# Optimization experiments

Measured on AMD Instinct MI355X. Metric: run time of the kernel, lower is better.

The kernel has to match this reference:

```python
import jax, jax.numpy as jnp
import numpy as np

T, B, X, F, Z, H = 64, 512, 784, 64, 64, 512


def _lin(v, W, b):
    return v @ W.T + b


def _gru(xt, h, Wih, Whh, bih, bhh):
    # PyTorch GRUCell gate math
    gi = xt @ Wih.T + bih
    gh = h @ Whh.T + bhh
    ir, iz, in_ = jnp.split(gi, 3, axis=-1)
    hr, hz, hn = jnp.split(gh, 3, axis=-1)
    r = jax.nn.sigmoid(ir + hr)
    z = jax.nn.sigmoid(iz + hz)
    n = jnp.tanh(in_ + r * hn)
    return (1.0 - z) * n + z * h


def _kld(mu1, sd1, mu2, sd2):
    r = sd1 / sd2
    return 0.5 * jnp.sum(((mu1 - mu2) / sd2) ** 2 + r ** 2 - 2.0 * jnp.log(r) - 1.0)


def setup_inputs() -> dict:
    key = jax.random.key(0)
    ks = iter(jax.random.split(key, 64))

    def Wn(*shape):
        return 0.02 * jax.random.normal(next(ks), shape, jnp.float32)

    d = {}
    d["x"] = jax.random.uniform(next(ks), (T, B, X), jnp.float32)
    d["eps_f"] = jax.random.normal(next(ks), (B, F), jnp.float32)
    d["eps_z"] = jax.random.normal(next(ks), (T, B, Z), jnp.float32)
    d.update(
        pxW1=Wn(H, X), pxb1=Wn(H), pxW2=Wn(H, H), pxb2=Wn(H),
        pzW=Wn(H, Z), pzb=Wn(H),
        pfW=Wn(H, F), pfb=Wn(H),
        rWih=Wn(3 * H, 3 * H), rWhh=Wn(3 * H, H), rbih=Wn(3 * H), rbhh=Wn(3 * H),
        zpW=Wn(H, H), zpb=Wn(H), zpmW=Wn(Z, H), zpmb=Wn(Z), zpsW=Wn(Z, H), zpsb=Wn(Z),
        feWih=Wn(3 * H, H), feWhh=Wn(3 * H, H), febih=Wn(3 * H), febhh=Wn(3 * H),
        femW=Wn(F, H), femb=Wn(F), fesW=Wn(F, H), fesb=Wn(F),
        zeW1=Wn(H, 2 * H), zeb1=Wn(H), zeW2=Wn(H, H), zeb2=Wn(H),
        zemW=Wn(Z, H), zemb=Wn(Z), zesW=Wn(Z, H), zesb=Wn(Z),
        dW1=Wn(H, 3 * H), db1=Wn(H), dW2=Wn(H, H), db2=Wn(H),
        dmW=Wn(X, H), dmb=Wn(X),
    )
    return d


def reference(x, eps_f, eps_z, pxW1, pxb1, pxW2, pxb2, pzW, pzb, pfW, pfb,
              rWih, rWhh, rbih, rbhh, zpW, zpb, zpmW, zpmb, zpsW, zpsb,
              feWih, feWhh, febih, febhh, femW, femb, fesW, fesb,
              zeW1, zeb1, zeW2, zeb2, zemW, zemb, zesW, zesb,
              dW1, db1, dW2, db2, dmW, dmb):
    relu = jax.nn.relu
    # phi_x over all timesteps at once: [T, B, H]
    phi_x = relu(_lin(relu(_lin(x, pxW1, pxb1)), pxW2, pxb2))
    h0 = jnp.zeros((x.shape[1], H), x.dtype)

    # f encoder GRU over the sequence; only the final hidden is used
    f_h, _ = jax.lax.scan(
        lambda h, xt: (_gru(xt, h, feWih, feWhh, febih, febhh), None), h0, phi_x)
    f_mean = _lin(f_h, femW, femb)
    f_std = jax.nn.softplus(_lin(f_h, fesW, fesb))
    f = eps_f * f_std + f_mean
    phi_f = relu(_lin(f, pfW, pfb))
    f_kld = _kld(f_mean, f_std, jnp.zeros_like(f_mean), jnp.ones_like(f_std))

    def step(carry, inp):
        h, zk, nll = carry
        px_t, e_t, x_t = inp
        zp = relu(_lin(h, zpW, zpb))
        zpm = _lin(zp, zpmW, zpmb)
        zps = jax.nn.softplus(_lin(zp, zpsW, zpsb))
        ze = relu(_lin(relu(_lin(jnp.concatenate([px_t, h], 1), zeW1, zeb1)), zeW2, zeb2))
        zem = _lin(ze, zemW, zemb)
        zes = jax.nn.softplus(_lin(ze, zesW, zesb))
        z_t = e_t * zes + zem
        phi_z = relu(_lin(z_t, pzW, pzb))
        dec = relu(_lin(relu(_lin(jnp.concatenate([phi_z, phi_f, h], 1), dW1, db1)), dW2, db2))
        dec_mean = jax.nn.sigmoid(_lin(dec, dmW, dmb))
        h_new = _gru(jnp.concatenate([px_t, phi_z, phi_f], 1), h, rWih, rWhh, rbih, rbhh)
        zk = zk + _kld(zem, zes, zpm, zps)
        nll = nll - jnp.sum(x_t * jnp.log(dec_mean) + (1.0 - x_t) * jnp.log(1.0 - dec_mean))
        return (h_new, zk, nll), None

    zero = jnp.zeros((), x.dtype)
    (_, z_kld, nll), _ = jax.lax.scan(step, (h0, zero, zero), (phi_x, eps_z, x))
    return (f_kld, z_kld, nll)
```

## Files before the change

### kernel.cpp

```cpp
#include <hip/hip_runtime.h>
#include <cmath>

namespace {

constexpr int Tn = 64;
constexpr int Bn = 512;
constexpr int Xn = 784;
constexpr int XnP = 800;
constexpr int Fn = 64;
constexpr int Zn = 64;
constexpr int Hn = 512;

typedef unsigned short us;
typedef __attribute__((ext_vector_type(8))) short bf16x8;
typedef __attribute__((ext_vector_type(4))) float f32x4;

__device__ __forceinline__ us f2b(float v) {
  unsigned int u = __float_as_uint(v);
  return (us)((u + 0x7FFFu + ((u >> 16) & 1u)) >> 16);
}
__device__ __forceinline__ float b2f(us u) { return __uint_as_float(((unsigned int)u) << 16); }
__device__ __forceinline__ float sigmf(float v) { return 1.0f / (1.0f + __expf(-v)); }
__device__ __forceinline__ float splusf(float v) {
  return v > 0.0f ? (v + log1pf(__expf(-v))) : log1pf(__expf(v));
}
__device__ __forceinline__ float block_sum(float v, float* red) {
  #pragma unroll
  for (int off = 32; off > 0; off >>= 1) v += __shfl_down(v, off, 64);
  if ((threadIdx.x & 63) == 0) red[threadIdx.x >> 6] = v;
  __syncthreads();
  float s = 0.0f;
  if (threadIdx.x == 0) s = red[0] + red[1] + red[2] + red[3];
  return s;
}

__global__ void cvt(const float* __restrict__ s, us* __restrict__ d, int n) {
  int i = blockIdx.x * 256 + threadIdx.x;
  if (i < n) d[i] = f2b(s[i]);
}
__global__ void cvt_pad(const float* __restrict__ s, us* __restrict__ d, int C, int Cp, int n) {
  int i = blockIdx.x * 256 + threadIdx.x;
  if (i < n) {
    int r = i / Cp, c = i - r * Cp;
    d[i] = (c < C) ? f2b(s[(size_t)r * C + c]) : (us)0;
  }
}

template <int NSEG, bool RELU, bool F32OUT, bool HASINIT, bool HASBIAS>
__device__ void tile_gemmx(
    int bx, int by,
    const us* A0, const us* W0, int ldw0, int K0,
    const us* A1, const us* W1, int ldw1, int K1,
    const float* initC, int ldi, const float* bias,
    void* Cout, int ldc, char* smemc)
{
  us* As = (us*)smemc; us* Bs = (us*)(smemc + 5120);
  const int tid = threadIdx.x, srow = tid >> 2, scb = (tid & 3) * 8;
  const int lane = tid & 63, w = tid >> 6, l15 = lane & 15, q = lane >> 4;
  const int m0 = by * 64, n0 = bx * 64;
  f32x4 acc[4];
  if (HASINIT) {
    #pragma unroll
    for (int j = 0; j < 4; ++j)
      #pragma unroll
      for (int r = 0; r < 4; ++r)
        acc[j][r] = initC[(size_t)(m0 + w * 16 + q * 4 + r) * ldi + n0 + j * 16 + l15];
  } else {
    #pragma unroll
    for (int j = 0; j < 4; ++j) acc[j] = (f32x4){0.f, 0.f, 0.f, 0.f};
  }
  #pragma unroll
  for (int seg = 0; seg < NSEG; ++seg) {
    const us* A = (seg == 0) ? A0 : A1;
    const us* W = (seg == 0) ? W0 : W1;
    const int ldw = (seg == 0) ? ldw0 : ldw1;
    const int K   = (seg == 0) ? K0 : K1;
    const us* ap = A + (size_t)(m0 + srow) * K + scb;
    const us* wp = W + (size_t)(n0 + srow) * ldw + scb;
    uint4 av = *(const uint4*)ap;
    uint4 wv = *(const uint4*)wp;
    for (int k0 = 0; k0 < K; k0 += 32) {
      __syncthreads();
      *(uint4*)&As[srow * 40 + scb] = av;
      *(uint4*)&Bs[srow * 40 + scb] = wv;
      __syncthreads();
      if (k0 + 32 < K) {
        av = *(const uint4*)(ap + k0 + 32);
        wv = *(const uint4*)(wp + k0 + 32);
      }
      bf16x8 a = *(const bf16x8*)&As[(w * 16 + l15) * 40 + q * 8];
      #pragma unroll
      for (int j = 0; j < 4; ++j) {
        bf16x8 b = *(const bf16x8*)&Bs[(j * 16 + l15) * 40 + q * 8];
        acc[j] = __builtin_amdgcn_mfma_f32_16x16x32_bf16(a, b, acc[j], 0, 0, 0);
      }
    }
  }
  #pragma unroll
  for (int j = 0; j < 4; ++j) {
    const int col = n0 + j * 16 + l15;
    const float bv = HASBIAS ? bias[col] : 0.f;
    #pragma unroll
    for (int r = 0; r < 4; ++r) {
      const int row = m0 + w * 16 + q * 4 + r;
      float v = acc[j][r] + bv;
      if (RELU) v = fmaxf(v, 0.f);
      if (F32OUT) ((float*)Cout)[(size_t)row * ldc + col] = v;
      else        ((us*)Cout)[(size_t)row * ldc + col] = f2b(v);
    }
  }
}

__device__ void tile_gru_fe(
    int bx, int by,
    const us* A0, const us* Wih,
    const us* hprev, const us* Whh,
    const float* bih, const float* bhh,
    us* hnew, char* smemc)
{
  us* Asm = (us*)smemc; us* Rs = (us*)(smemc + 5120);
  us* Zs = (us*)(smemc + 10240); us* Ns = (us*)(smemc + 15360);
  const int tid = threadIdx.x, srow = tid >> 2, scb = (tid & 3) * 8;
  const int lane = tid & 63, w = tid >> 6, l15 = lane & 15, q = lane >> 4;
  const int m0 = by * 64, c0 = bx * 64;
  f32x4 aR[4], aZ[4], aI[4], aH[4];
  #pragma unroll
  for (int j = 0; j < 4; ++j) {
    aR[j] = (f32x4){0.f, 0.f, 0.f, 0.f}; aZ[j] = aR[j]; aI[j] = aR[j]; aH[j] = aR[j];
  }
  #pragma unroll
  for (int seg = 0; seg < 2; ++seg) {
    const bool hseg = (seg == 1);
    const us* A  = hseg ? hprev : A0;
    const us* Wb = hseg ? Whh : Wih;
    const us* ap = A + (size_t)(m0 + srow) * Hn + scb;
    const us* wr = Wb + (size_t)(c0 + srow) * Hn + scb;
    const us* wz = wr + (size_t)Hn * Hn;
    const us* wn = wz + (size_t)Hn * Hn;
    uint4 av = *(const uint4*)ap;
    uint4 rv = *(const uint4*)wr;
    uint4 zv = *(const uint4*)wz;
    uint4 nv = *(const uint4*)wn;
    for (int k0 = 0; k0 < Hn; k0 += 32) {
      __syncthreads();
      *(uint4*)&Asm[srow * 40 + scb] = av;
      *(uint4*)&Rs[srow * 40 + scb] = rv;
      *(uint4*)&Zs[srow * 40 + scb] = zv;
      *(uint4*)&Ns[srow * 40 + scb] = nv;
      __syncthreads();
      if (k0 + 32 < Hn) {
        av = *(const uint4*)(ap + k0 + 32);
        rv = *(const uint4*)(wr + k0 + 32);
        zv = *(const uint4*)(wz + k0 + 32);
        nv = *(const uint4*)(wn + k0 + 32);
      }
      bf16x8 a = *(const bf16x8*)&Asm[(w * 16 + l15) * 40 + q * 8];
      #pragma unroll
      for (int j = 0; j < 4; ++j) {
        bf16x8 br = *(const bf16x8*)&Rs[(j * 16 + l15) * 40 + q * 8];
        bf16x8 bz = *(const bf16x8*)&Zs[(j * 16 + l15) * 40 + q * 8];
        bf16x8 bn = *(const bf16x8*)&Ns[(j * 16 + l15) * 40 + q * 8];
        aR[j] = __builtin_amdgcn_mfma_f32_16x16x32_bf16(a, br, aR[j], 0, 0, 0);
        aZ[j] = __builtin_amdgcn_mfma_f32_16x16x32_bf16(a, bz, aZ[j], 0, 0, 0);
        if (hseg) aH[j] = __builtin_amdgcn_mfma_f32_16x16x32_bf16(a, bn, aH[j], 0, 0, 0);
        else      aI[j] = __builtin_amdgcn_mfma_f32_16x16x32_bf16(a, bn, aI[j], 0, 0, 0);
      }
    }
  }
  #pragma unroll
  for (int j = 0; j < 4; ++j) {
    const int c = c0 + j * 16 + l15;
    const float bR = bih[c] + bhh[c];
    const float bZ = bih[Hn + c] + bhh[Hn + c];
    const float bI = bih[2 * Hn + c];
    const float bH = bhh[2 * Hn + c];
    #pragma unroll
    for (int r = 0; r < 4; ++r) {
      const int m = m0 + w * 16 + q * 4 + r;
      const float h = b2f(hprev[(size_t)m * Hn + c]);
      const float rg = sigmf(aR[j][r] + bR);
      const float zg = sigmf(aZ[j][r] + bZ);
      const float ng = tanhf(aI[j][r] + bI + rg * (aH[j][r] + bH));
      hnew[(size_t)m * Hn + c] = f2b((1.0f - zg) * ng + zg * h);
    }
  }
}

__device__ void tile_gru_fin(
    int bx, int by,
    const us* phiz, const us* rWih,
    const float* gipre, const float* ghpre,
    const us* hprev,
    const float* bih, const float* bhh,
    us* hnew, char* smemc)
{
  us* Asm = (us*)smemc; us* Rs = (us*)(smemc + 5120);
  us* Zs = (us*)(smemc + 10240); us* Ns = (us*)(smemc + 15360);
  const int tid = threadIdx.x, srow = tid >> 2, scb = (tid & 3) * 8;
  const int lane = tid & 63, w = tid >> 6, l15 = lane & 15, q = lane >> 4;
  const int m0 = by * 64, c0 = bx * 64;
  f32x4 aR[4], aZ[4], aI[4];
  float aH[4][4];
  #pragma unroll
  for (int j = 0; j < 4; ++j) {
    const int c = c0 + j * 16 + l15;
    #pragma unroll
    for (int r = 0; r < 4; ++r) {
      const size_t row = (size_t)(m0 + w * 16 + q * 4 + r) * 1536;
      aR[j][r] = gipre[row + c] + ghpre[row + c];
      aZ[j][r] = gipre[row + 512 + c] + ghpre[row + 512 + c];
      aI[j][r] = gipre[row + 1024 + c];
      aH[j][r] = ghpre[row + 1024 + c];
    }
  }
  const us* ap = phiz + (size_t)(m0 + srow) * Hn + scb;
  const us* wr = rWih + (size_t)(c0 + srow) * 1536 + 512 + scb;
  const us* wz = wr + (size_t)512 * 1536;
  const us* wn = wz + (size_t)512 * 1536;
  uint4 av = *(const uint4*)ap;
  uint4 rv = *(const uint4*)wr;
  uint4 zv = *(const uint4*)wz;
  uint4 nv = *(const uint4*)wn;
  for (int k0 = 0; k0 < Hn; k0 += 32) {
    __syncthreads();
    *(uint4*)&Asm[srow * 40 + scb] = av;
    *(uint4*)&Rs[srow * 40 + scb] = rv;
    *(uint4*)&Zs[srow * 40 + scb] = zv;
    *(uint4*)&Ns[srow * 40 + scb] = nv;
    __syncthreads();
    if (k0 + 32 < Hn) {
      av = *(const uint4*)(ap + k0 + 32);
      rv = *(const uint4*)(wr + k0 + 32);
      zv = *(const uint4*)(wz + k0 + 32);
      nv = *(const uint4*)(wn + k0 + 32);
    }
    bf16x8 a = *(const bf16x8*)&Asm[(w * 16 + l15) * 40 + q * 8];
    #pragma unroll
    for (int j = 0; j < 4; ++j) {
      bf16x8 br = *(const bf16x8*)&Rs[(j * 16 + l15) * 40 + q * 8];
      bf16x8 bz = *(const bf16x8*)&Zs[(j * 16 + l15) * 40 + q * 8];
      bf16x8 bn = *(const bf16x8*)&Ns[(j * 16 + l15) * 40 + q * 8];
      aR[j] = __builtin_amdgcn_mfma_f32_16x16x32_bf16(a, br, aR[j], 0, 0, 0);
      aZ[j] = __builtin_amdgcn_mfma_f32_16x16x32_bf16(a, bz, aZ[j], 0, 0, 0);
      aI[j] = __builtin_amdgcn_mfma_f32_16x16x32_bf16(a, bn, aI[j], 0, 0, 0);
    }
  }
  #pragma unroll
  for (int j = 0; j < 4; ++j) {
    const int c = c0 + j * 16 + l15;
    const float bR = bih[c] + bhh[c];
    const float bZ = bih[Hn + c] + bhh[Hn + c];
    const float bI = bih[2 * Hn + c];
    const float bH = bhh[2 * Hn + c];
    #pragma unroll
    for (int r = 0; r < 4; ++r) {
      const int m = m0 + w * 16 + q * 4 + r;
      const float h = b2f(hprev[(size_t)m * Hn + c]);
      const float rg = sigmf(aR[j][r] + bR);
      const float zg = sigmf(aZ[j][r] + bZ);
      const float ng = tanhf(aI[j][r] + bI + rg * (aH[j][r] + bH));
      hnew[(size_t)m * Hn + c] = f2b((1.0f - zg) * ng + zg * h);
    }
  }
}

__device__ void tile_nll(
    int bx, int by,
    const us* dec, const us* dmW, const float* dmb, const float* xt,
    float* nll, char* smemc)
{
  us* As = (us*)smemc; us* Bs = (us*)(smemc + 5120);
  float* red = (float*)(smemc + 10240);
  const int tid = threadIdx.x, srow = tid >> 2, scb = (tid & 3) * 8;
  const int lane = tid & 63, w = tid >> 6, l15 = lane & 15, q = lane >> 4;
  const int m0 = by * 64, n0 = bx * 64;
  f32x4 acc[4];
  #pragma unroll
  for (int j = 0; j < 4; ++j) acc[j] = (f32x4){0.f, 0.f, 0.f, 0.f};
  const int wrow = (n0 + srow < Xn) ? (n0 + srow) : (Xn - 1);
  const us* ap = dec + (size_t)(m0 + srow) * Hn + scb;
  const us* wp = dmW + (size_t)wrow * Hn + scb;
  uint4 av = *(const uint4*)ap;
  uint4 wv = *(const uint4*)wp;
  for (int k0 = 0; k0 < Hn; k0 += 32) {
    __syncthreads();
    *(uint4*)&As[srow * 40 + scb] = av;
    *(uint4*)&Bs[srow * 40 + scb] = wv;
    __syncthreads();
    if (k0 + 32 < Hn) {
      av = *(const uint4*)(ap + k0 + 32);
      wv = *(const uint4*)(wp + k0 + 32);
    }
    bf16x8 a = *(const bf16x8*)&As[(w * 16 + l15) * 40 + q * 8];
    #pragma unroll
    for (int j = 0; j < 4; ++j) {
      bf16x8 b = *(const bf16x8*)&Bs[(j * 16 + l15) * 40 + q * 8];
      acc[j] = __builtin_amdgcn_mfma_f32_16x16x32_bf16(a, b, acc[j], 0, 0, 0);
    }
  }
  float sum = 0.0f;
  #pragma unroll
  for (int j = 0; j < 4; ++j) {
    const int n = n0 + j * 16 + l15;
    if (n < Xn) {
      const float bv = dmb[n];
      #pragma unroll
      for (int r = 0; r < 4; ++r) {
        const int m = m0 + w * 16 + q * 4 + r;
        const float a = acc[j][r] + bv;
        const float xv = xt[(size_t)m * Xn + n];
        sum += splusf(-a) + (1.0f - xv) * a;
      }
    }
  }
  const float s = block_sum(sum, red);
  if (tid == 0) atomicAdd(nll, s);
}

template <int MODE>
__device__ void stat_dual(int vb,
    const us* Ain, const us* Wm, const float* bm, const us* Ws, const float* bs,
    const float* eps, const float* pm_in, const float* ps_in,
    us* o0b, float* o_pm, float* o_ps, float* kacc, char* smemc)
{
  us* As = (us*)smemc; us* Ms = (us*)(smemc + 5120); us* Ss = (us*)(smemc + 10240);
  float* red = (float*)(smemc + 15360);
  const int tid = threadIdx.x, srow = tid >> 2, scb = (tid & 3) * 8;
  const int lane = tid & 63, w = tid >> 6, l15 = lane & 15, q = lane >> 4;
  const int m0 = vb * 64;
  f32x4 am[4], as_[4];
  #pragma unroll
  for (int j = 0; j < 4; ++j) { am[j] = (f32x4){0.f, 0.f, 0.f, 0.f}; as_[j] = am[j]; }
  const us* ap = Ain + (size_t)(m0 + srow) * Hn + scb;
  const us* mp = Wm + (size_t)srow * Hn + scb;
  const us* sp = Ws + (size_t)srow * Hn + scb;
  uint4 av = *(const uint4*)ap;
  uint4 mv = *(const uint4*)mp;
  uint4 sv = *(const uint4*)sp;
  for (int k0 = 0; k0 < Hn; k0 += 32) {
    __syncthreads();
    *(uint4*)&As[srow * 40 + scb] = av;
    *(uint4*)&Ms[srow * 40 + scb] = mv;
    *(uint4*)&Ss[srow * 40 + scb] = sv;
    __syncthreads();
    if (k0 + 32 < Hn) {
      av = *(const uint4*)(ap + k0 + 32);
      mv = *(const uint4*)(mp + k0 + 32);
      sv = *(const uint4*)(sp + k0 + 32);
    }
    bf16x8 a = *(const bf16x8*)&As[(w * 16 + l15) * 40 + q * 8];
    #pragma unroll
    for (int j = 0; j < 4; ++j) {
      bf16x8 b0 = *(const bf16x8*)&Ms[(j * 16 + l15) * 40 + q * 8];
      bf16x8 b1 = *(const bf16x8*)&Ss[(j * 16 + l15) * 40 + q * 8];
      am[j]  = __builtin_amdgcn_mfma_f32_16x16x32_bf16(a, b0, am[j], 0, 0, 0);
      as_[j] = __builtin_amdgcn_mfma_f32_16x16x32_bf16(a, b1, as_[j], 0, 0, 0);
    }
  }
  float kld = 0.0f;
  #pragma unroll
  for (int j = 0; j < 4; ++j) {
    const int c = j * 16 + l15;
    const float bmv = bm[c], bsv = bs[c];
    #pragma unroll
    for (int r = 0; r < 4; ++r) {
      const int m = m0 + w * 16 + q * 4 + r;
      const float mu = am[j][r] + bmv;
      const float sd = splusf(as_[j][r] + bsv);
      if (MODE == 0) {
        o_pm[(size_t)m * Zn + c] = mu;
        o_ps[(size_t)m * Zn + c] = sd;
      } else {
        o0b[(size_t)m * Zn + c] = f2b(eps[(size_t)m * Zn + c] * sd + mu);
        if (MODE == 1) {
          kld += mu * mu + sd * sd - 2.0f * __logf(sd) - 1.0f;
        } else {
          const float pm = pm_in[(size_t)m * Zn + c];
          const float ps = ps_in[(size_t)m * Zn + c];
          const float dd = (mu - pm) / ps;
          const float rr = sd / ps;
          kld += dd * dd + rr * rr - 2.0f * __logf(rr) - 1.0f;
        }
      }
    }
  }
  if (MODE != 0) {
    const float s = block_sum(kld, red);
    if (tid == 0) atomicAdd(kacc, 0.5f * s);
  }
}

__global__ __launch_bounds__(256) void k_gemmA(
    const us* A, const us* W, int ldw, int K, const float* bias, us* C, int ldc)
{
  __shared__ alignas(16) char sm[10240];
  tile_gemmx<1, true, false, false, true>(blockIdx.x, blockIdx.y, A, W, ldw, K,
      nullptr, nullptr, 0, 0, nullptr, 0, bias, C, ldc, sm);
}

__global__ __launch_bounds__(256) void k_gruB(
    const us* A0, const us* Wih, const us* hprev, const us* Whh,
    const float* bih, const float* bhh, us* hnew)
{
  __shared__ alignas(16) char sm[20480];
  tile_gru_fe(blockIdx.x, blockIdx.y, A0, Wih, hprev, Whh, bih, bhh, hnew, sm);
}

__global__ __launch_bounds__(256) void k_statf(
    const us* fh, const us* femW, const float* femb, const us* fesW, const float* fesb,
    const float* eps_f, us* fbuf, float* kacc)
{
  __shared__ alignas(16) char sm[15376];
  stat_dual<1>(blockIdx.x, fh, femW, femb, fesW, fesb, eps_f,
               nullptr, nullptr, fbuf, nullptr, nullptr, kacc, sm);
}

__global__ __launch_bounds__(256) void kP2(
    const us* phi_f, const us* rWih, const us* dW1, const float* db1,
    float* Cpre_gru, float* Cpre_dec)
{
  __shared__ alignas(16) char sm[10240];
  const int b = blockIdx.x;
  if (b < 192)
    tile_gemmx<1, false, true, false, false>(b % 24, b / 24, phi_f, rWih + 1024, 1536, Hn,
        nullptr, nullptr, 0, 0, nullptr, 0, nullptr, Cpre_gru, 1536, sm);
  else
    tile_gemmx<1, false, true, false, true>((b - 192) & 7, (b - 192) >> 3,
        phi_f, dW1 + 512, 1536, Hn,
        nullptr, nullptr, 0, 0, nullptr, 0, db1, Cpre_dec, 512, sm);
}

__global__ __launch_bounds__(256) void kP3(
    const us* h0, const us* zpW, const float* zpb, us* zp,
    const us* px0, const us* zeW1, const float* zeb1, us* zepre)
{
  __shared__ alignas(16) char sm[10240];
  const int b = blockIdx.x;
  if (b < 64)
    tile_gemmx<1, true, false, false, true>(b & 7, b >> 3, h0, zpW, Hn, Hn,
        nullptr, nullptr, 0, 0, nullptr, 0, zpb, zp, Hn, sm);
  else
    tile_gemmx<2, true, false, false, true>((b - 64) & 7, (b - 64) >> 3,
        px0, zeW1, 1024, Hn, h0, zeW1 + 512, 1024, Hn,
        nullptr, 0, zeb1, zepre, Hn, sm);
}

__global__ __launch_bounds__(256) void kP4(
    const us* zepre, const us* zeW2, const float* zeb2, us* ze,
    const us* zp, const us* zpmW, const float* zpmb, const us* zpsW, const float* zpsb,
    float* zpm, float* zps)
{
  __shared__ alignas(16) char sm[15376];
  const int b = blockIdx.x;
  if (b < 64)
    tile_gemmx<1, true, false, false, true>(b & 7, b >> 3, zepre, zeW2, Hn, Hn,
        nullptr, nullptr, 0, 0, nullptr, 0, zeb2, ze, Hn, sm);
  else
    stat_dual<0>(b - 64, zp, zpmW, zpmb, zpsW, zpsb,
                 nullptr, nullptr, nullptr, nullptr, zpm, zps, nullptr, sm);
}

__global__ __launch_bounds__(256) void kS1(
    const us* ze, const us* zemW, const float* zemb, const us* zesW, const float* zesb,
    const float* eps_zt, const float* zpm, const float* zps, us* zt, float* kacc,
    const us* px_t, const us* rWih, const float* Cpre_gru, float* gipre)
{
  __shared__ alignas(16) char sm[15376];
  const int b = blockIdx.x;
  if (b < 8)
    stat_dual<2>(b, ze, zemW, zemb, zesW, zesb, eps_zt, zpm, zps,
                 zt, nullptr, nullptr, kacc, sm);
  else {
    const int tb = b - 8;
    tile_gemmx<1, false, true, true, false>(tb % 24, tb / 24, px_t, rWih, 1536, Hn,
        nullptr, nullptr, 0, 0, Cpre_gru, 1536, nullptr, gipre, 1536, sm);
  }
}

__global__ __launch_bounds__(256) void kS2(
    const us* zt, const us* pzW, const float* pzb, us* phiz)
{
  __shared__ alignas(16) char sm[10240];
  tile_gemmx<1, true, false, false, true>(blockIdx.x & 7, blockIdx.x >> 3, zt, pzW, Zn, Zn,
      nullptr, nullptr, 0, 0, nullptr, 0, pzb, phiz, Hn, sm);
}

__global__ __launch_bounds__(256) void kS3(
    const us* phiz, const us* rWih, const float* gipre, const float* ghpre,
    const us* hprev, const float* rbih, const float* rbhh, us* hnew,
    const us* dW1, const float* dtmph, us* dtmp)
{
  __shared__ alignas(16) char sm[20480];
  const int b = blockIdx.x;
  if (b < 64)
    tile_gru_fin(b & 7, b >> 3, phiz, rWih, gipre, ghpre, hprev, rbih, rbhh, hnew, sm);
  else
    tile_gemmx<1, true, false, true, false>((b - 64) & 7, (b - 64) >> 3, phiz, dW1, 1536, Hn,
        nullptr, nullptr, 0, 0, dtmph, 512, nullptr, dtmp, Hn, sm);
}

__global__ __launch_bounds__(256) void kS4(
    const us* dtmp, const us* dW2, const float* db2, us* dec,
    const us* hnext, const us* zpW, const float* zpb, us* zp,
    const us* px1, const us* zeW1, const float* zeb1, us* zepre,
    const us* dW1, const float* Cpre_dec, float* dtmph)
{
  __shared__ alignas(16) char sm[10240];
  const int b = blockIdx.x;
  if (b < 64)
    tile_gemmx<1, true, false, false, true>(b & 7, b >> 3, dtmp, dW2, Hn, Hn,
        nullptr, nullptr, 0, 0, nullptr, 0, db2, dec, Hn, sm);
  else if (b < 128)
    tile_gemmx<1, true, false, false, true>((b - 64) & 7, (b - 64) >> 3, hnext, zpW, Hn, Hn,
        nullptr, nullptr, 0, 0, nullptr, 0, zpb, zp, Hn, sm);
  else if (b < 192)
    tile_gemmx<2, true, false, false, true>((b - 128) & 7, (b - 128) >> 3,
        px1, zeW1, 1024, Hn, hnext, zeW1 + 512, 1024, Hn,
        nullptr, 0, zeb1, zepre, Hn, sm);
  else
    tile_gemmx<1, false, true, true, false>((b - 192) & 7, (b - 192) >> 3,
        hnext, dW1 + 1024, 1536, Hn,
        nullptr, nullptr, 0, 0, Cpre_dec, 512, nullptr, dtmph, 512, sm);
}

__global__ __launch_bounds__(256) void kS5(
    const us* dec, const us* dmW, const float* dmb, const float* xt, float* nll,
    const us* zepre, const us* zeW2, const float* zeb2, us* ze,
    const us* zp, const us* zpmW, const float* zpmb, const us* zpsW, const float* zpsb,
    float* zpm, float* zps,
    const us* hnext, const us* rWhh, float* ghpre)
{
  __shared__ alignas(16) char sm[15376];
  const int b = blockIdx.x;
  if (b < 104)
    tile_nll(b % 13, b / 13, dec, dmW, dmb, xt, nll, sm);
  else if (b < 168)
    tile_gemmx<1, true, false, false, true>((b - 104) & 7, (b - 104) >> 3, zepre, zeW2, Hn, Hn,
        nullptr, nullptr, 0, 0, nullptr, 0, zeb2, ze, Hn, sm);
  else if (b < 176)
    stat_dual<0>(b - 168, zp, zpmW, zpmb, zpsW, zpsb,
                 nullptr, nullptr, nullptr, nullptr, zpm, zps, nullptr, sm);
  else {
    const int tb = b - 176;
    tile_gemmx<1, false, true, false, false>(tb % 24, tb / 24, hnext, rWhh, Hn, Hn,
        nullptr, nullptr, 0, 0, nullptr, 0, nullptr, ghpre, 1536, sm);
  }
}

}

extern "C" void kernel_launch(void* const* d_in, const int* in_sizes, int n_in,
                              void* d_out, int out_size, void* d_ws, size_t ws_size,
                              hipStream_t stream)
{
  (void)in_sizes; (void)n_in; (void)out_size;
  const float* x     = (const float*)d_in[0];
  const float* eps_f = (const float*)d_in[1];
  const float* eps_z = (const float*)d_in[2];
  const float* pxW1  = (const float*)d_in[3];
  const float* pxb1  = (const float*)d_in[4];
  const float* pxW2  = (const float*)d_in[5];
  const float* pxb2  = (const float*)d_in[6];
  const float* pzW   = (const float*)d_in[7];
  const float* pzb   = (const float*)d_in[8];
  const float* pfW   = (const float*)d_in[9];
  const float* pfb   = (const float*)d_in[10];
  const float* rWih  = (const float*)d_in[11];
  const float* rWhh  = (const float*)d_in[12];
  const float* rbih  = (const float*)d_in[13];
  const float* rbhh  = (const float*)d_in[14];
  const float* zpW   = (const float*)d_in[15];
  const float* zpb   = (const float*)d_in[16];
  const float* zpmW  = (const float*)d_in[17];
  const float* zpmb  = (const float*)d_in[18];
  const float* zpsW  = (const float*)d_in[19];
  const float* zpsb  = (const float*)d_in[20];
  const float* feWih = (const float*)d_in[21];
  const float* feWhh = (const float*)d_in[22];
  const float* febih = (const float*)d_in[23];
  const float* febhh = (const float*)d_in[24];
  const float* femW  = (const float*)d_in[25];
  const float* femb  = (const float*)d_in[26];
  const float* fesW  = (const float*)d_in[27];
  const float* fesb  = (const float*)d_in[28];
  const float* zeW1  = (const float*)d_in[29];
  const float* zeb1  = (const float*)d_in[30];
  const float* zeW2  = (const float*)d_in[31];
  const float* zeb2  = (const float*)d_in[32];
  const float* zemW  = (const float*)d_in[33];
  const float* zemb  = (const float*)d_in[34];
  const float* zesW  = (const float*)d_in[35];
  const float* zesb  = (const float*)d_in[36];
  const float* dW1   = (const float*)d_in[37];
  const float* db1   = (const float*)d_in[38];
  const float* dW2   = (const float*)d_in[39];
  const float* db2   = (const float*)d_in[40];
  const float* dmW   = (const float*)d_in[41];
  const float* dmb   = (const float*)d_in[42];
  float* out = (float*)d_out;

  char* base = (char*)d_ws;
  size_t off = 0;
  auto ab = [&](size_t bytes) -> void* {
    void* p = base + off;
    off += (bytes + 255) & ~(size_t)255;
    return p;
  };

  us* b_pxW1  = (us*)ab((size_t)512 * XnP * 2);
  us* b_pxW2  = (us*)ab((size_t)512 * 512 * 2);
  us* b_pzW   = (us*)ab((size_t)512 * 64 * 2);
  us* b_pfW   = (us*)ab((size_t)512 * 64 * 2);
  us* b_rWih  = (us*)ab((size_t)1536 * 1536 * 2);
  us* b_rWhh  = (us*)ab((size_t)1536 * 512 * 2);
  us* b_zpW   = (us*)ab((size_t)512 * 512 * 2);
  us* b_zpmW  = (us*)ab((size_t)64 * 512 * 2);
  us* b_zpsW  = (us*)ab((size_t)64 * 512 * 2);
  us* b_feWih = (us*)ab((size_t)1536 * 512 * 2);
  us* b_feWhh = (us*)ab((size_t)1536 * 512 * 2);
  us* b_femW  = (us*)ab((size_t)64 * 512 * 2);
  us* b_fesW  = (us*)ab((size_t)64 * 512 * 2);
  us* b_zeW1  = (us*)ab((size_t)512 * 1024 * 2);
  us* b_zeW2  = (us*)ab((size_t)512 * 512 * 2);
  us* b_zemW  = (us*)ab((size_t)64 * 512 * 2);
  us* b_zesW  = (us*)ab((size_t)64 * 512 * 2);
  us* b_dW1   = (us*)ab((size_t)512 * 1536 * 2);
  us* b_dW2   = (us*)ab((size_t)512 * 512 * 2);
  us* b_dmW   = (us*)ab((size_t)Xn * 512 * 2);

  us* phi_x = (us*)ab((size_t)Tn * Bn * Hn * 2);
  us* fh_a  = (us*)ab((size_t)Bn * Hn * 2);
  us* h_a   = (us*)ab((size_t)Bn * Hn * 2);
  us* fh_b  = (us*)ab((size_t)Bn * Hn * 2);
  us* h_b   = (us*)ab((size_t)Bn * Hn * 2);
  us* fbuf  = (us*)ab((size_t)Bn * Fn * 2);
  us* phi_f = (us*)ab((size_t)Bn * Hn * 2);
  us* zp    = (us*)ab((size_t)Bn * Hn * 2);
  us* zepre = (us*)ab((size_t)Bn * Hn * 2);
  us* ze    = (us*)ab((size_t)Bn * Hn * 2);
  us* zt    = (us*)ab((size_t)Bn * Zn * 2);
  us* phiz  = (us*)ab((size_t)Bn * Hn * 2);
  us* dtmp  = (us*)ab((size_t)Bn * Hn * 2);
  us* dec   = (us*)ab((size_t)Bn * Hn * 2);
  float* zpm = (float*)ab((size_t)Bn * Zn * 4);
  float* zps = (float*)ab((size_t)Bn * Zn * 4);
  float* Cpre_gru = (float*)ab((size_t)Bn * 1536 * 4);
  float* Cpre_dec = (float*)ab((size_t)Bn * 512 * 4);
  float* gipre    = (float*)ab((size_t)Bn * 1536 * 4);
  float* ghpre    = (float*)ab((size_t)Bn * 1536 * 4);
  float* dtmph    = (float*)ab((size_t)Bn * 512 * 4);

  int CH = 16;
  while (CH > 1 && off + (size_t)CH * (Bn * XnP + Bn * Hn) * 2 + 4096 > ws_size) CH >>= 1;
  us* xch  = (us*)ab((size_t)CH * Bn * XnP * 2);
  us* tmpb = (us*)ab((size_t)CH * Bn * Hn * 2);

  hipMemsetAsync(d_out, 0, 3 * sizeof(float), stream);
  hipMemsetAsync(fh_a, 0, 2 * (size_t)Bn * Hn * 2, stream);
  hipMemsetAsync(ghpre, 0, (size_t)Bn * 1536 * 4, stream);

  const dim3 blk(256);
  auto CVT = [&](const float* s, us* d, size_t n) {
    cvt<<<dim3((unsigned)((n + 255) / 256)), blk, 0, stream>>>(s, d, (int)n);
  };

  {
    const size_t n = (size_t)512 * XnP;
    cvt_pad<<<dim3((unsigned)((n + 255) / 256)), blk, 0, stream>>>(pxW1, b_pxW1, Xn, XnP, (int)n);
  }
  CVT(pxW2, b_pxW2, (size_t)512 * 512);
  CVT(pzW, b_pzW, (size_t)512 * 64);
  CVT(pfW, b_pfW, (size_t)512 * 64);
  CVT(rWih, b_rWih, (size_t)1536 * 1536);
  CVT(rWhh, b_rWhh, (size_t)1536 * 512);
  CVT(zpW, b_zpW, (size_t)512 * 512);
  CVT(zpmW, b_zpmW, (size_t)64 * 512);
  CVT(zpsW, b_zpsW, (size_t)64 * 512);
  CVT(feWih, b_feWih, (size_t)1536 * 512);
  CVT(feWhh, b_feWhh, (size_t)1536 * 512);
  CVT(femW, b_femW, (size_t)64 * 512);
  CVT(fesW, b_fesW, (size_t)64 * 512);
  CVT(zeW1, b_zeW1, (size_t)512 * 1024);
  CVT(zeW2, b_zeW2, (size_t)512 * 512);
  CVT(zemW, b_zemW, (size_t)64 * 512);
  CVT(zesW, b_zesW, (size_t)64 * 512);
  CVT(dW1, b_dW1, (size_t)512 * 1536);
  CVT(dW2, b_dW2, (size_t)512 * 512);
  CVT(dmW, b_dmW, (size_t)Xn * 512);

  for (int c = 0; c < Tn / CH; ++c) {
    const size_t nx = (size_t)CH * Bn * XnP;
    cvt_pad<<<dim3((unsigned)((nx + 255) / 256)), blk, 0, stream>>>(
        x + (size_t)c * CH * Bn * Xn, xch, Xn, XnP, (int)nx);
    const dim3 gA(8, CH * Bn / 64);
    k_gemmA<<<gA, blk, 0, stream>>>(xch, b_pxW1, XnP, XnP, pxb1, tmpb, Hn);
    k_gemmA<<<gA, blk, 0, stream>>>(tmpb, b_pxW2, Hn, Hn, pxb2,
                                    phi_x + (size_t)c * CH * Bn * Hn, Hn);
  }

  us* fc = fh_a; us* fn2 = fh_b;
  for (int t = 0; t < Tn; ++t) {
    k_gruB<<<dim3(8, 8), blk, 0, stream>>>(
        phi_x + (size_t)t * Bn * Hn, b_feWih, fc, b_feWhh, febih, febhh, fn2);
    us* sw = fc; fc = fn2; fn2 = sw;
  }

  k_statf<<<dim3(8), blk, 0, stream>>>(fh_a, b_femW, femb, b_fesW, fesb, eps_f, fbuf, out + 0);

  k_gemmA<<<dim3(8, 8), blk, 0, stream>>>(fbuf, b_pfW, Fn, Fn, pfb, phi_f, Hn);
  kP2<<<dim3(256), blk, 0, stream>>>(phi_f, b_rWih, b_dW1, db1, Cpre_gru, Cpre_dec);
  hipMemcpyAsync(dtmph, Cpre_dec, (size_t)Bn * 512 * 4, hipMemcpyDeviceToDevice, stream);
  kP3<<<dim3(128), blk, 0, stream>>>(h_a, b_zpW, zpb, zp, phi_x, b_zeW1, zeb1, zepre);
  kP4<<<dim3(72), blk, 0, stream>>>(zepre, b_zeW2, zeb2, ze,
                                    zp, b_zpmW, zpmb, b_zpsW, zpsb, zpm, zps);

  for (int t = 0; t < Tn; ++t) {
    const us* hcur = (t & 1) ? h_b : h_a;
    us* hnext      = (t & 1) ? h_a : h_b;
    const bool last = (t == Tn - 1);
    const us* px_t = phi_x + (size_t)t * Bn * Hn;

    kS1<<<dim3(200), blk, 0, stream>>>(
        ze, b_zemW, zemb, b_zesW, zesb, eps_z + (size_t)t * Bn * Zn, zpm, zps,
        zt, out + 1, px_t, b_rWih, Cpre_gru, gipre);

    kS2<<<dim3(64), blk, 0, stream>>>(zt, b_pzW, pzb, phiz);

    kS3<<<dim3(128), blk, 0, stream>>>(
        phiz, b_rWih, gipre, ghpre, hcur, rbih, rbhh, hnext,
        b_dW1, dtmph, dtmp);

    kS4<<<dim3(last ? 64 : 256), blk, 0, stream>>>(
        dtmp, b_dW2, db2, dec,
        hnext, b_zpW, zpb, zp,
        phi_x + (size_t)(t + 1) * Bn * Hn, b_zeW1, zeb1, zepre,
        b_dW1, Cpre_dec, dtmph);

    kS5<<<dim3(last ? 104 : 368), blk, 0, stream>>>(
        dec, b_dmW, dmb, x + (size_t)t * Bn * Xn, out + 2,
        zepre, b_zeW2, zeb2, ze,
        zp, b_zpmW, zpmb, b_zpsW, zpsb, zpm, zps,
        hnext, b_rWhh, ghpre);
  }
}
```

Before: 6.594 ms.

## Replace per-step kernel launches with a single cooperative persistent megakernel

Folds the weight conversion, phi_x GEMMs, f-encoder GRU and the whole 64-step recurrence into one cooperative kernel of 256 blocks. Grid-wide syncs replace the hundreds of separate kernel launches. The GRU is split so the input-side gate GEMM is precomputed separately from the hidden-side GEMM. The NLL reconstruction term is moved out of the recurrence into one batched kernel over all timesteps, which appears to reuse the phi_x buffer to hold the decoder outputs. Grid.sync cost and the fixed one-block-per-CU occupancy could offset the removed launch overhead.

After: 16.11 ms. 2.44x slower.

```diff
diff --git a/kernel.cpp b/kernel.cpp
--- a/kernel.cpp
+++ b/kernel.cpp
@@ -1,5 +1,8 @@
 #include <hip/hip_runtime.h>
+#include <hip/hip_cooperative_groups.h>
 #include <cmath>
+
+namespace cg = cooperative_groups;
 
 namespace {
 
@@ -10,6 +13,8 @@
 constexpr int Fn = 64;
 constexpr int Zn = 64;
 constexpr int Hn = 512;
+constexpr int NB = 256;
+constexpr int NTH = 256;
 
 typedef unsigned short us;
 typedef __attribute__((ext_vector_type(8))) short bf16x8;
@@ -34,17 +39,27 @@
   return s;
 }
 
-__global__ void cvt(const float* __restrict__ s, us* __restrict__ d, int n) {
-  int i = blockIdx.x * 256 + threadIdx.x;
-  if (i < n) d[i] = f2b(s[i]);
-}
-__global__ void cvt_pad(const float* __restrict__ s, us* __restrict__ d, int C, int Cp, int n) {
-  int i = blockIdx.x * 256 + threadIdx.x;
-  if (i < n) {
-    int r = i / Cp, c = i - r * Cp;
-    d[i] = (c < C) ? f2b(s[(size_t)r * C + c]) : (us)0;
-  }
-}
+struct KParams {
+  const float *x, *eps_f, *eps_z;
+  const float *f_pxW1, *pxb1, *f_pxW2, *pxb2;
+  const float *f_pzW, *pzb, *f_pfW, *pfb;
+  const float *f_rWih, *f_rWhh, *rbih, *rbhh;
+  const float *f_zpW, *zpb, *f_zpmW, *zpmb, *f_zpsW, *zpsb;
+  const float *f_feWih, *f_feWhh, *febih, *febhh;
+  const float *f_femW, *femb, *f_fesW, *fesb;
+  const float *f_zeW1, *zeb1, *f_zeW2, *zeb2, *f_zemW, *zemb, *f_zesW, *zesb;
+  const float *f_dW1, *db1, *f_dW2, *db2, *f_dmW, *dmb;
+  float* out;
+  us *b_pxW1, *b_pxW2, *b_pzW, *b_pfW, *b_rWih, *b_rWhh, *b_zpW, *b_zpmW, *b_zpsW;
+  us *b_feWih, *b_feWhh, *b_femW, *b_fesW, *b_zeW1, *b_zeW2, *b_zemW, *b_zesW;
+  us *b_dW1, *b_dW2, *b_dmW;
+  us *phi_x, *fh_a, *fh_b, *fbuf, *phi_f, *h_a, *h_b;
+  us *zp, *zepre, *ze, *phiz, *dtmp, *dec;
+  float *zpm, *zps, *Cpre_gru, *Cpre_dec, *gipre, *ghpre, *dtmph;
+  float *parts;
+  us *xch, *tmpb;
+  int CH;
+};
 
 template <int NSEG, bool RELU, bool F32OUT, bool HASINIT, bool HASBIAS>
 __device__ void tile_gemmx(
@@ -111,60 +126,122 @@
   }
 }
 
-__device__ void tile_gru_fe(
-    int bx, int by,
-    const us* A0, const us* Wih,
-    const us* hprev, const us* Whh,
-    const float* bih, const float* bhh,
-    us* hnew, char* smemc)
+template <bool HASINIT>
+__device__ void tile_g3(int bx, int by, const us* A, const us* W, int ldw,
+                        const float* initC, float* outC, char* smemc)
 {
   us* Asm = (us*)smemc; us* Rs = (us*)(smemc + 5120);
   us* Zs = (us*)(smemc + 10240); us* Ns = (us*)(smemc + 15360);
   const int tid = threadIdx.x, srow = tid >> 2, scb = (tid & 3) * 8;
   const int lane = tid & 63, w = tid >> 6, l15 = lane & 15, q = lane >> 4;
   const int m0 = by * 64, c0 = bx * 64;
-  f32x4 aR[4], aZ[4], aI[4], aH[4];
+  f32x4 aR[4], aZ[4], aN[4];
+  if (HASINIT) {
+    #pragma unroll
+    for (int j = 0; j < 4; ++j) {
+      const int c = c0 + j * 16 + l15;
+      #pragma unroll
+      for (int r = 0; r < 4; ++r) {
+        const size_t row = (size_t)(m0 + w * 16 + q * 4 + r) * 1536;
+        aR[j][r] = initC[row + c];
+        aZ[j][r] = initC[row + 512 + c];
+        aN[j][r] = initC[row + 1024 + c];
+      }
+    }
+  } else {
+    #pragma unroll
+    for (int j = 0; j < 4; ++j) {
+      aR[j] = (f32x4){0.f, 0.f, 0.f, 0.f}; aZ[j] = aR[j]; aN[j] = aR[j];
+    }
+  }
+  const us* ap = A + (size_t)(m0 + srow) * Hn + scb;
+  const us* wr = W + (size_t)(c0 + srow) * ldw + scb;
+  const us* wz = wr + (size_t)512 * ldw;
+  const us* wn = wz + (size_t)512 * ldw;
+  uint4 av = *(const uint4*)ap;
+  uint4 rv = *(const uint4*)wr;
+  uint4 zv = *(const uint4*)wz;
+  uint4 nv = *(const uint4*)wn;
+  for (int k0 = 0; k0 < Hn; k0 += 32) {
+    __syncthreads();
+    *(uint4*)&Asm[srow * 40 + scb] = av;
+    *(uint4*)&Rs[srow * 40 + scb] = rv;
+    *(uint4*)&Zs[srow * 40 + scb] = zv;
+    *(uint4*)&Ns[srow * 40 + scb] = nv;
+    __syncthreads();
+    if (k0 + 32 < Hn) {
+      av = *(const uint4*)(ap + k0 + 32);
+      rv = *(const uint4*)(wr + k0 + 32);
+      zv = *(const uint4*)(wz + k0 + 32);
+      nv = *(const uint4*)(wn + k0 + 32);
+    }
+    bf16x8 a = *(const bf16x8*)&Asm[(w * 16 + l15) * 40 + q * 8];
+    #pragma unroll
+    for (int j = 0; j < 4; ++j) {
+      bf16x8 br = *(const bf16x8*)&Rs[(j * 16 + l15) * 40 + q * 8];
+      bf16x8 bz = *(const bf16x8*)&Zs[(j * 16 + l15) * 40 + q * 8];
+      bf16x8 bn = *(const bf16x8*)&Ns[(j * 16 + l15) * 40 + q * 8];
+      aR[j] = __builtin_amdgcn_mfma_f32_16x16x32_bf16(a, br, aR[j], 0, 0, 0);
+      aZ[j] = __builtin_amdgcn_mfma_f32_16x16x32_bf16(a, bz, aZ[j], 0, 0, 0);
+      aN[j] = __builtin_amdgcn_mfma_f32_16x16x32_bf16(a, bn, aN[j], 0, 0, 0);
+    }
+  }
   #pragma unroll
   for (int j = 0; j < 4; ++j) {
-    aR[j] = (f32x4){0.f, 0.f, 0.f, 0.f}; aZ[j] = aR[j]; aI[j] = aR[j]; aH[j] = aR[j];
-  }
-  #pragma unroll
-  for (int seg = 0; seg < 2; ++seg) {
-    const bool hseg = (seg == 1);
-    const us* A  = hseg ? hprev : A0;
-    const us* Wb = hseg ? Whh : Wih;
-    const us* ap = A + (size_t)(m0 + srow) * Hn + scb;
-    const us* wr = Wb + (size_t)(c0 + srow) * Hn + scb;
-    const us* wz = wr + (size_t)Hn * Hn;
-    const us* wn = wz + (size_t)Hn * Hn;
-    uint4 av = *(const uint4*)ap;
-    uint4 rv = *(const uint4*)wr;
-    uint4 zv = *(const uint4*)wz;
-    uint4 nv = *(const uint4*)wn;
-    for (int k0 = 0; k0 < Hn; k0 += 32) {
-      __syncthreads();
-      *(uint4*)&Asm[srow * 40 + scb] = av;
-      *(uint4*)&Rs[srow * 40 + scb] = rv;
-      *(uint4*)&Zs[srow * 40 + scb] = zv;
-      *(uint4*)&Ns[srow * 40 + scb] = nv;
-      __syncthreads();
-      if (k0 + 32 < Hn) {
-        av = *(const uint4*)(ap + k0 + 32);
-        rv = *(const uint4*)(wr + k0 + 32);
-        zv = *(const uint4*)(wz + k0 + 32);
-        nv = *(const uint4*)(wn + k0 + 32);
-      }
-      bf16x8 a = *(const bf16x8*)&Asm[(w * 16 + l15) * 40 + q * 8];
-      #pragma unroll
-      for (int j = 0; j < 4; ++j) {
-        bf16x8 br = *(const bf16x8*)&Rs[(j * 16 + l15) * 40 + q * 8];
-        bf16x8 bz = *(const bf16x8*)&Zs[(j * 16 + l15) * 40 + q * 8];
-        bf16x8 bn = *(const bf16x8*)&Ns[(j * 16 + l15) * 40 + q * 8];
-        aR[j] = __builtin_amdgcn_mfma_f32_16x16x32_bf16(a, br, aR[j], 0, 0, 0);
-        aZ[j] = __builtin_amdgcn_mfma_f32_16x16x32_bf16(a, bz, aZ[j], 0, 0, 0);
-        if (hseg) aH[j] = __builtin_amdgcn_mfma_f32_16x16x32_bf16(a, bn, aH[j], 0, 0, 0);
-        else      aI[j] = __builtin_amdgcn_mfma_f32_16x16x32_bf16(a, bn, aI[j], 0, 0, 0);
-      }
+    const int c = c0 + j * 16 + l15;
+    #pragma unroll
+    for (int r = 0; r < 4; ++r) {
+      const size_t row = (size_t)(m0 + w * 16 + q * 4 + r) * 1536;
+      outC[row + c] = aR[j][r];
+      outC[row + 512 + c] = aZ[j][r];
+      outC[row + 1024 + c] = aN[j][r];
+    }
+  }
+}
+
+__device__ void tile_ghgates(int bx, int by, const us* hprev, const us* Whh,
+    const float* gi, const float* bih, const float* bhh, us* hnew, char* smemc)
+{
+  us* Asm = (us*)smemc; us* Rs = (us*)(smemc + 5120);
+  us* Zs = (us*)(smemc + 10240); us* Ns = (us*)(smemc + 15360);
+  const int tid = threadIdx.x, srow = tid >> 2, scb = (tid & 3) * 8;
+  const int lane = tid & 63, w = tid >> 6, l15 = lane & 15, q = lane >> 4;
+  const int m0 = by * 64, c0 = bx * 64;
+  f32x4 aR[4], aZ[4], aH[4];
+  #pragma unroll
+  for (int j = 0; j < 4; ++j) {
+    aR[j] = (f32x4){0.f, 0.f, 0.f, 0.f}; aZ[j] = aR[j]; aH[j] = aR[j];
+  }
+  const us* ap = hprev + (size_t)(m0 + srow) * Hn + scb;
+  const us* wr = Whh + (size_t)(c0 + srow) * Hn + scb;
+  const us* wz = wr + (size_t)512 * Hn;
+  const us* wn = wz + (size_t)512 * Hn;
+  uint4 av = *(const uint4*)ap;
+  uint4 rv = *(const uint4*)wr;
+  uint4 zv = *(const uint4*)wz;
+  uint4 nv = *(const uint4*)wn;
+  for (int k0 = 0; k0 < Hn; k0 += 32) {
+    __syncthreads();
+    *(uint4*)&Asm[srow * 40 + scb] = av;
+    *(uint4*)&Rs[srow * 40 + scb] = rv;
+    *(uint4*)&Zs[srow * 40 + scb] = zv;
+    *(uint4*)&Ns[srow * 40 + scb] = nv;
+    __syncthreads();
+    if (k0 + 32 < Hn) {
+      av = *(const uint4*)(ap + k0 + 32);
+      rv = *(const uint4*)(wr + k0 + 32);
+      zv = *(const uint4*)(wz + k0 + 32);
+      nv = *(const uint4*)(wn + k0 + 32);
+    }
+    bf16x8 a = *(const bf16x8*)&Asm[(w * 16 + l15) * 40 + q * 8];
+    #pragma unroll
+    for (int j = 0; j < 4; ++j) {
+      bf16x8 br = *(const bf16x8*)&Rs[(j * 16 + l15) * 40 + q * 8];
+      bf16x8 bz = *(const bf16x8*)&Zs[(j * 16 + l15) * 40 + q * 8];
+      bf16x8 bn = *(const bf16x8*)&Ns[(j * 16 + l15) * 40 + q * 8];
+      aR[j] = __builtin_amdgcn_mfma_f32_16x16x32_bf16(a, br, aR[j], 0, 0, 0);
+      aZ[j] = __builtin_amdgcn_mfma_f32_16x16x32_bf16(a, bz, aZ[j], 0, 0, 0);
+      aH[j] = __builtin_amdgcn_mfma_f32_16x16x32_bf16(a, bn, aH[j], 0, 0, 0);
     }
   }
   #pragma unroll
@@ -177,10 +254,11 @@
     #pragma unroll
     for (int r = 0; r < 4; ++r) {
       const int m = m0 + w * 16 + q * 4 + r;
+      const size_t grow = (size_t)m * 1536;
       const float h = b2f(hprev[(size_t)m * Hn + c]);
-      const float rg = sigmf(aR[j][r] + bR);
-      const float zg = sigmf(aZ[j][r] + bZ);
-      const float ng = tanhf(aI[j][r] + bI + rg * (aH[j][r] + bH));
+      const float rg = sigmf(gi[grow + c] + aR[j][r] + bR);
+      const float zg = sigmf(gi[grow + 512 + c] + aZ[j][r] + bZ);
+      const float ng = tanhf(gi[grow + 1024 + c] + bI + rg * (aH[j][r] + bH));
       hnew[(size_t)m * Hn + c] = f2b((1.0f - zg) * ng + zg * h);
     }
   }
@@ -264,11 +342,356 @@
   }
 }
 
-__device__ void tile_nll(
-    int bx, int by,
-    const us* dec, const us* dmW, const float* dmb, const float* xt,
-    float* nll, char* smemc)
+template <int MODE>
+__device__ float stat_dual(int vb,
+    const us* Ain, const us* Wm, const float* bm, const us* Ws, const float* bs,
+    const float* eps,
+    us* o0b, float* o_pm, float* o_ps, char* smemc)
 {
+  us* As = (us*)smemc; us* Ms = (us*)(smemc + 5120); us* Ss = (us*)(smemc + 10240);
+  float* red = (float*)(smemc + 15360);
+  const int tid = threadIdx.x, srow = tid >> 2, scb = (tid & 3) * 8;
+  const int lane = tid & 63, w = tid >> 6, l15 = lane & 15, q = lane >> 4;
+  const int m0 = vb * 64;
+  f32x4 am[4], as_[4];
+  #pragma unroll
+  for (int j = 0; j < 4; ++j) { am[j] = (f32x4){0.f, 0.f, 0.f, 0.f}; as_[j] = am[j]; }
+  const us* ap = Ain + (size_t)(m0 + srow) * Hn + scb;
+  const us* mp = Wm + (size_t)srow * Hn + scb;
+  const us* sp = Ws + (size_t)srow * Hn + scb;
+  uint4 av = *(const uint4*)ap;
+  uint4 mv = *(const uint4*)mp;
+  uint4 sv = *(const uint4*)sp;
+  for (int k0 = 0; k0 < Hn; k0 += 32) {
+    __syncthreads();
+    *(uint4*)&As[srow * 40 + scb] = av;
+    *(uint4*)&Ms[srow * 40 + scb] = mv;
+    *(uint4*)&Ss[srow * 40 + scb] = sv;
+    __syncthreads();
+    if (k0 + 32 < Hn) {
+      av = *(const uint4*)(ap + k0 + 32);
+      mv = *(const uint4*)(mp + k0 + 32);
+      sv = *(const uint4*)(sp + k0 + 32);
+    }
+    bf16x8 a = *(const bf16x8*)&As[(w * 16 + l15) * 40 + q * 8];
+    #pragma unroll
+    for (int j = 0; j < 4; ++j) {
+      bf16x8 b0 = *(const bf16x8*)&Ms[(j * 16 + l15) * 40 + q * 8];
+      bf16x8 b1 = *(const bf16x8*)&Ss[(j * 16 + l15) * 40 + q * 8];
+      am[j]  = __builtin_amdgcn_mfma_f32_16x16x32_bf16(a, b0, am[j], 0, 0, 0);
+      as_[j] = __builtin_amdgcn_mfma_f32_16x16x32_bf16(a, b1, as_[j], 0, 0, 0);
+    }
+  }
+  float kld = 0.0f;
+  #pragma unroll
+  for (int j = 0; j < 4; ++j) {
+    const int c = j * 16 + l15;
+    const float bmv = bm[c], bsv = bs[c];
+    #pragma unroll
+    for (int r = 0; r < 4; ++r) {
+      const int m = m0 + w * 16 + q * 4 + r;
+      const float mu = am[j][r] + bmv;
+      const float sd = splusf(as_[j][r] + bsv);
+      if (MODE == 0) {
+        o_pm[(size_t)m * Zn + c] = mu;
+        o_ps[(size_t)m * Zn + c] = sd;
+      } else {
+        o0b[(size_t)m * Zn + c] = f2b(eps[(size_t)m * Zn + c] * sd + mu);
+        kld += mu * mu + sd * sd - 2.0f * __logf(sd) - 1.0f;
+      }
+    }
+  }
+  if (MODE != 0) return 0.5f * block_sum(kld, red);
+  return 0.0f;
+}
+
+__device__ float tile_zestat_phiz(int vb,
+    const us* ze, const us* Wm, const float* bm, const us* Ws, const float* bs,
+    const float* eps, const float* pm_in, const float* ps_in,
+    const us* pzW, const float* pzb, us* phiz,
+    char* smemc)
+{
+  us* As = (us*)smemc; us* Ms = (us*)(smemc + 5120); us* Ss = (us*)(smemc + 10240);
+  float* red = (float*)(smemc + 15360);
+  const int tid = threadIdx.x, srow = tid >> 2, scb = (tid & 3) * 8;
+  const int lane = tid & 63, w = tid >> 6, l15 = lane & 15, q = lane >> 4;
+  const int m0 = vb * 64;
+  f32x4 am[4], as_[4];
+  #pragma unroll
+  for (int j = 0; j < 4; ++j) { am[j] = (f32x4){0.f, 0.f, 0.f, 0.f}; as_[j] = am[j]; }
+  const us* ap = ze + (size_t)(m0 + srow) * Hn + scb;
+  const us* mp = Wm + (size_t)srow * Hn + scb;
+  const us* sp = Ws + (size_t)srow * Hn + scb;
+  uint4 av = *(const uint4*)ap;
+  uint4 mv = *(const uint4*)mp;
+  uint4 sv = *(const uint4*)sp;
+  for (int k0 = 0; k0 < Hn; k0 += 32) {
+    __syncthreads();
+    *(uint4*)&As[srow * 40 + scb] = av;
+    *(uint4*)&Ms[srow * 40 + scb] = mv;
+    *(uint4*)&Ss[srow * 40 + scb] = sv;
+    __syncthreads();
+    if (k0 + 32 < Hn) {
+      av = *(const uint4*)(ap + k0 + 32);
+      mv = *(const uint4*)(mp + k0 + 32);
+      sv = *(const uint4*)(sp + k0 + 32);
+    }
+    bf16x8 a = *(const bf16x8*)&As[(w * 16 + l15) * 40 + q * 8];
+    #pragma unroll
+    for (int j = 0; j < 4; ++j) {
+      bf16x8 b0 = *(const bf16x8*)&Ms[(j * 16 + l15) * 40 + q * 8];
+      bf16x8 b1 = *(const bf16x8*)&Ss[(j * 16 + l15) * 40 + q * 8];
+      am[j]  = __builtin_amdgcn_mfma_f32_16x16x32_bf16(a, b0, am[j], 0, 0, 0);
+      as_[j] = __builtin_amdgcn_mfma_f32_16x16x32_bf16(a, b1, as_[j], 0, 0, 0);
+    }
+  }
+  float kld = 0.0f;
+  us ztv[4][4];
+  #pragma unroll
+  for (int j = 0; j < 4; ++j) {
+    const int c = j * 16 + l15;
+    const float bmv = bm[c], bsv = bs[c];
+    #pragma unroll
+    for (int r = 0; r < 4; ++r) {
+      const int m = m0 + w * 16 + q * 4 + r;
+      const float mu = am[j][r] + bmv;
+      const float sd = splusf(as_[j][r] + bsv);
+      ztv[j][r] = f2b(eps[(size_t)m * Zn + c] * sd + mu);
+      const float pm = pm_in[(size_t)m * Zn + c];
+      const float ps = ps_in[(size_t)m * Zn + c];
+      const float dd = (mu - pm) / ps;
+      const float rr = sd / ps;
+      kld += dd * dd + rr * rr - 2.0f * __logf(rr) - 1.0f;
+    }
+  }
+  const float kout = 0.5f * block_sum(kld, red);
+  us* zts = (us*)smemc;
+  us* Bs = (us*)(smemc + 10240);
+  #pragma unroll
+  for (int j = 0; j < 4; ++j)
+    #pragma unroll
+    for (int r = 0; r < 4; ++r)
+      zts[(w * 16 + q * 4 + r) * 72 + (j * 16 + l15)] = ztv[j][r];
+  for (int nt = 0; nt < 8; ++nt) {
+    f32x4 pa[4];
+    #pragma unroll
+    for (int j = 0; j < 4; ++j) pa[j] = (f32x4){0.f, 0.f, 0.f, 0.f};
+    const us* wp = pzW + (size_t)(nt * 64 + srow) * 64 + scb;
+    uint4 wv = *(const uint4*)wp;
+    for (int k0 = 0; k0 < 64; k0 += 32) {
+      __syncthreads();
+      *(uint4*)&Bs[srow * 40 + scb] = wv;
+      __syncthreads();
+      if (k0 == 0) wv = *(const uint4*)(wp + 32);
+      bf16x8 a = *(const bf16x8*)&zts[(w * 16 + l15) * 72 + k0 + q * 8];
+      #pragma unroll
+      for (int j = 0; j < 4; ++j) {
+        bf16x8 b = *(const bf16x8*)&Bs[(j * 16 + l15) * 40 + q * 8];
+        pa[j] = __builtin_amdgcn_mfma_f32_16x16x32_bf16(a, b, pa[j], 0, 0, 0);
+      }
+    }
+    #pragma unroll
+    for (int j = 0; j < 4; ++j) {
+      const int col = nt * 64 + j * 16 + l15;
+      const float bv = pzb[col];
+      #pragma unroll
+      for (int r = 0; r < 4; ++r) {
+        const int row = m0 + w * 16 + q * 4 + r;
+        phiz[(size_t)row * Hn + col] = f2b(fmaxf(pa[j][r] + bv, 0.f));
+      }
+    }
+  }
+  return kout;
+}
+
+__global__ __launch_bounds__(NTH, 1) void k_mega(KParams p)
+{
+  cg::grid_group grid = cg::this_grid();
+  __shared__ alignas(16) char sm[20496];
+  const int bid = blockIdx.x;
+  const int gtid = bid * NTH + threadIdx.x;
+  const int gnt = NB * NTH;
+
+  {
+    const float* srcs[19] = {p.f_pxW2, p.f_pzW, p.f_pfW, p.f_rWih, p.f_rWhh,
+        p.f_zpW, p.f_zpmW, p.f_zpsW, p.f_feWih, p.f_feWhh, p.f_femW, p.f_fesW,
+        p.f_zeW1, p.f_zeW2, p.f_zemW, p.f_zesW, p.f_dW1, p.f_dW2, p.f_dmW};
+    us* dsts[19] = {p.b_pxW2, p.b_pzW, p.b_pfW, p.b_rWih, p.b_rWhh,
+        p.b_zpW, p.b_zpmW, p.b_zpsW, p.b_feWih, p.b_feWhh, p.b_femW, p.b_fesW,
+        p.b_zeW1, p.b_zeW2, p.b_zemW, p.b_zesW, p.b_dW1, p.b_dW2, p.b_dmW};
+    const int ns[19] = {512*512, 512*64, 512*64, 1536*1536, 1536*512,
+        512*512, 64*512, 64*512, 1536*512, 1536*512, 64*512, 64*512,
+        512*1024, 512*512, 64*512, 64*512, 512*1536, 512*512, 784*512};
+    for (int k = 0; k < 19; ++k) {
+      const float* s = srcs[k]; us* d = dsts[k]; const int n = ns[k];
+      for (int i = gtid; i < n; i += gnt) d[i] = f2b(s[i]);
+    }
+  }
+  for (int i = gtid; i < 512 * XnP; i += gnt) {
+    const int r = i / XnP, c = i - r * XnP;
+    p.b_pxW1[i] = (c < Xn) ? f2b(p.f_pxW1[(size_t)r * Xn + c]) : (us)0;
+  }
+  for (int i = gtid; i < Bn * Hn; i += gnt) { p.fh_a[i] = 0; p.h_a[i] = 0; }
+  for (int i = gtid; i < Bn * 1536; i += gnt) p.ghpre[i] = 0.f;
+  grid.sync();
+
+  const int CH = p.CH;
+  const int nch = Tn / CH;
+  for (int c = 0; c < nch; ++c) {
+    const int nx = CH * Bn * XnP;
+    const float* xsrc = p.x + (size_t)c * CH * Bn * Xn;
+    for (int i = gtid; i < nx; i += gnt) {
+      const int r = i / XnP, cc = i - r * XnP;
+      p.xch[i] = (cc < Xn) ? f2b(xsrc[(size_t)r * Xn + cc]) : (us)0;
+    }
+    grid.sync();
+    const int ntile = (CH * Bn / 64) * 8;
+    for (int tl = bid; tl < ntile; tl += NB)
+      tile_gemmx<1, true, false, false, true>(tl & 7, tl >> 3, p.xch, p.b_pxW1,
+          XnP, XnP, nullptr, nullptr, 0, 0, nullptr, 0, p.pxb1, p.tmpb, Hn, sm);
+    grid.sync();
+    for (int tl = bid; tl < ntile; tl += NB)
+      tile_gemmx<1, true, false, false, true>(tl & 7, tl >> 3, p.tmpb, p.b_pxW2,
+          Hn, Hn, nullptr, nullptr, 0, 0, nullptr, 0, p.pxb2,
+          p.phi_x + (size_t)c * CH * Bn * Hn, Hn, sm);
+    grid.sync();
+  }
+
+  float* giA = p.Cpre_gru;
+  float* giB = p.gipre;
+  if (bid < 64)
+    tile_g3<false>(bid & 7, bid >> 3, p.phi_x, p.b_feWih, Hn, nullptr, giA, sm);
+  grid.sync();
+  for (int t = 0; t < Tn; ++t) {
+    const us* hc = (t & 1) ? p.fh_b : p.fh_a;
+    us* hn = (t & 1) ? p.fh_a : p.fh_b;
+    const float* gic = (t & 1) ? giB : giA;
+    float* gin = (t & 1) ? giA : giB;
+    if (bid < 64)
+      tile_ghgates(bid & 7, bid >> 3, hc, p.b_feWhh, gic, p.febih, p.febhh, hn, sm);
+    else if (bid < 128 && t + 1 < Tn)
+      tile_g3<false>((bid - 64) & 7, (bid - 64) >> 3,
+          p.phi_x + (size_t)(t + 1) * Bn * Hn, p.b_feWih, Hn, nullptr, gin, sm);
+    grid.sync();
+  }
+
+  if (bid < 8) {
+    const float fk = stat_dual<1>(bid, p.fh_a, p.b_femW, p.femb, p.b_fesW, p.fesb,
+                                  p.eps_f, p.fbuf, nullptr, nullptr, sm);
+    if (threadIdx.x == 0) p.parts[8 + bid] = fk;
+  } else if (bid < 72)
+    tile_gemmx<1, true, false, false, true>((bid - 8) & 7, (bid - 8) >> 3,
+        p.phi_x, p.b_zeW1, 1024, Hn, nullptr, nullptr, 0, 0,
+        nullptr, 0, p.zeb1, p.zepre, Hn, sm);
+  else {
+    for (int i = (bid - 72) * NTH + threadIdx.x; i < Bn * Hn; i += (NB - 72) * NTH)
+      p.zp[i] = f2b(fmaxf(p.zpb[i & (Hn - 1)], 0.f));
+  }
+  grid.sync();
+
+  if (bid < 64)
+    tile_gemmx<1, true, false, false, true>(bid & 7, bid >> 3, p.fbuf, p.b_pfW,
+        Fn, Fn, nullptr, nullptr, 0, 0, nullptr, 0, p.pfb, p.phi_f, Hn, sm);
+  else if (bid < 128)
+    tile_gemmx<1, true, false, false, true>((bid - 64) & 7, (bid - 64) >> 3,
+        p.zepre, p.b_zeW2, Hn, Hn, nullptr, nullptr, 0, 0,
+        nullptr, 0, p.zeb2, p.ze, Hn, sm);
+  else if (bid < 136)
+    stat_dual<0>(bid - 128, p.zp, p.b_zpmW, p.zpmb, p.b_zpsW, p.zpsb, nullptr,
+                 nullptr, p.zpm, p.zps, sm);
+  grid.sync();
+
+  if (bid < 64)
+    tile_g3<false>(bid & 7, bid >> 3, p.phi_f, p.b_rWih + 1024, 1536,
+                   nullptr, p.Cpre_gru, sm);
+  else if (bid < 128)
+    tile_gemmx<1, false, true, false, true>((bid - 64) & 7, (bid - 64) >> 3,
+        p.phi_f, p.b_dW1 + 512, 1536, Hn, nullptr, nullptr, 0, 0,
+        nullptr, 0, p.db1, p.Cpre_dec, 512, sm);
+  grid.sync();
+
+  float accZ = 0.f;
+  for (int t = 0; t < Tn; ++t) {
+    const us* hc = (t & 1) ? p.h_b : p.h_a;
+    us* hn = (t & 1) ? p.h_a : p.h_b;
+    const us* px_t = p.phi_x + (size_t)t * Bn * Hn;
+
+    if (bid < 8)
+      accZ += tile_zestat_phiz(bid, p.ze, p.b_zemW, p.zemb, p.b_zesW, p.zesb,
+          p.eps_z + (size_t)t * Bn * Zn, p.zpm, p.zps,
+          p.b_pzW, p.pzb, p.phiz, sm);
+    else if (bid < 72)
+      tile_g3<true>((bid - 8) & 7, (bid - 8) >> 3, px_t, p.b_rWih, 1536,
+                    p.Cpre_gru, p.gipre, sm);
+    grid.sync();
+
+    if (bid < 64)
+      tile_gru_fin(bid & 7, bid >> 3, p.phiz, p.b_rWih, p.gipre, p.ghpre, hc,
+                   p.rbih, p.rbhh, hn, sm);
+    else if (bid < 128)
+      tile_gemmx<1, true, false, true, false>((bid - 64) & 7, (bid - 64) >> 3,
+          p.phiz, p.b_dW1, 1536, Hn, nullptr, nullptr, 0, 0,
+          (t == 0 ? p.Cpre_dec : p.dtmph), 512, nullptr, p.dtmp, Hn, sm);
+    grid.sync();
+
+    if (bid < 64)
+      tile_gemmx<1, true, false, false, true>(bid & 7, bid >> 3, p.dtmp, p.b_dW2,
+          Hn, Hn, nullptr, nullptr, 0, 0, nullptr, 0, p.db2,
+          p.phi_x + (size_t)t * Bn * Hn, Hn, sm);
+    else if (bid < 128) {
+      if (t + 1 < Tn)
+        tile_gemmx<1, true, false, false, true>((bid - 64) & 7, (bid - 64) >> 3,
+            hn, p.b_zpW, Hn, Hn, nullptr, nullptr, 0, 0,
+            nullptr, 0, p.zpb, p.zp, Hn, sm);
+    } else if (bid < 192) {
+      if (t + 1 < Tn)
+        tile_gemmx<2, true, false, false, true>((bid - 128) & 7, (bid - 128) >> 3,
+            p.phi_x + (size_t)(t + 1) * Bn * Hn, p.b_zeW1, 1024, Hn,
+            hn, p.b_zeW1 + 512, 1024, Hn,
+            nullptr, 0, p.zeb1, p.zepre, Hn, sm);
+    } else {
+      if (t + 1 < Tn)
+        tile_gemmx<1, false, true, true, false>((bid - 192) & 7, (bid - 192) >> 3,
+            hn, p.b_dW1 + 1024, 1536, Hn, nullptr, nullptr, 0, 0,
+            p.Cpre_dec, 512, nullptr, p.dtmph, 512, sm);
+    }
+    grid.sync();
+
+    if (t + 1 < Tn) {
+      if (bid < 64)
+        tile_gemmx<1, true, false, false, true>(bid & 7, bid >> 3, p.zepre,
+            p.b_zeW2, Hn, Hn, nullptr, nullptr, 0, 0,
+            nullptr, 0, p.zeb2, p.ze, Hn, sm);
+      else if (bid < 72)
+        stat_dual<0>(bid - 64, p.zp, p.b_zpmW, p.zpmb, p.b_zpsW, p.zpsb, nullptr,
+                     nullptr, p.zpm, p.zps, sm);
+      else if (bid < 136)
+        tile_g3<false>((bid - 72) & 7, (bid - 72) >> 3, hn, p.b_rWhh, Hn,
+                       nullptr, p.ghpre, sm);
+    }
+    grid.sync();
+  }
+
+  if (threadIdx.x == 0 && bid < 8) p.parts[bid] = accZ;
+  grid.sync();
+  if (bid == 0 && threadIdx.x == 0) {
+    float f = 0.f, z = 0.f;
+    for (int i = 0; i < 8; ++i) { z += p.parts[i]; f += p.parts[8 + i]; }
+    p.out[0] = f; p.out[1] = z;
+  }
+}
+
+__global__ __launch_bounds__(NTH) void k_nll_all(
+    const us* dec_all, const us* dmW, const float* dmb, const float* x, float* nll)
+{
+  __shared__ alignas(16) char smemc[10256];
+  const int b = blockIdx.x;
+  const int t = b / 104;
+  const int i = b - t * 104;
+  const int bx = i % 13, by = i / 13;
+  const us* dec = dec_all + (size_t)t * Bn * Hn;
+  const float* xt = x + (size_t)t * Bn * Xn;
+
   us* As = (us*)smemc; us* Bs = (us*)(smemc + 5120);
   float* red = (float*)(smemc + 10240);
   const int tid = threadIdx.x, srow = tid >> 2, scb = (tid & 3) * 8;
@@ -294,8 +717,8 @@
     bf16x8 a = *(const bf16x8*)&As[(w * 16 + l15) * 40 + q * 8];
     #pragma unroll
     for (int j = 0; j < 4; ++j) {
-      bf16x8 b = *(const bf16x8*)&Bs[(j * 16 + l15) * 40 + q * 8];
-      acc[j] = __builtin_amdgcn_mfma_f32_16x16x32_bf16(a, b, acc[j], 0, 0, 0);
+      bf16x8 bb = *(const bf16x8*)&Bs[(j * 16 + l15) * 40 + q * 8];
+      acc[j] = __builtin_amdgcn_mfma_f32_16x16x32_bf16(a, bb, acc[j], 0, 0, 0);
     }
   }
   float sum = 0.0f;
@@ -317,236 +740,6 @@
   if (tid == 0) atomicAdd(nll, s);
 }
 
-template <int MODE>
-__device__ void stat_dual(int vb,
-    const us* Ain, const us* Wm, const float* bm, const us* Ws, const float* bs,
-    const float* eps, const float* pm_in, const float* ps_in,
-    us* o0b, float* o_pm, float* o_ps, float* kacc, char* smemc)
-{
-  us* As = (us*)smemc; us* Ms = (us*)(smemc + 5120); us* Ss = (us*)(smemc + 10240);
-  float* red = (float*)(smemc + 15360);
-  const int tid = threadIdx.x, srow = tid >> 2, scb = (tid & 3) * 8;
-  const int lane = tid & 63, w = tid >> 6, l15 = lane & 15, q = lane >> 4;
-  const int m0 = vb * 64;
-  f32x4 am[4], as_[4];
-  #pragma unroll
-  for (int j = 0; j < 4; ++j) { am[j] = (f32x4){0.f, 0.f, 0.f, 0.f}; as_[j] = am[j]; }
-  const us* ap = Ain + (size_t)(m0 + srow) * Hn + scb;
-  const us* mp = Wm + (size_t)srow * Hn + scb;
-  const us* sp = Ws + (size_t)srow * Hn + scb;
-  uint4 av = *(const uint4*)ap;
-  uint4 mv = *(const uint4*)mp;
-  uint4 sv = *(const uint4*)sp;
-  for (int k0 = 0; k0 < Hn; k0 += 32) {
-    __syncthreads();
-    *(uint4*)&As[srow * 40 + scb] = av;
-    *(uint4*)&Ms[srow * 40 + scb] = mv;
-    *(uint4*)&Ss[srow * 40 + scb] = sv;
-    __syncthreads();
-    if (k0 + 32 < Hn) {
-      av = *(const uint4*)(ap + k0 + 32);
-      mv = *(const uint4*)(mp + k0 + 32);
-      sv = *(const uint4*)(sp + k0 + 32);
-    }
-    bf16x8 a = *(const bf16x8*)&As[(w * 16 + l15) * 40 + q * 8];
-    #pragma unroll
-    for (int j = 0; j < 4; ++j) {
-      bf16x8 b0 = *(const bf16x8*)&Ms[(j * 16 + l15) * 40 + q * 8];
-      bf16x8 b1 = *(const bf16x8*)&Ss[(j * 16 + l15) * 40 + q * 8];
-      am[j]  = __builtin_amdgcn_mfma_f32_16x16x32_bf16(a, b0, am[j], 0, 0, 0);
-      as_[j] = __builtin_amdgcn_mfma_f32_16x16x32_bf16(a, b1, as_[j], 0, 0, 0);
-    }
-  }
-  float kld = 0.0f;
-  #pragma unroll
-  for (int j = 0; j < 4; ++j) {
-    const int c = j * 16 + l15;
-    const float bmv = bm[c], bsv = bs[c];
-    #pragma unroll
-    for (int r = 0; r < 4; ++r) {
-      const int m = m0 + w * 16 + q * 4 + r;
-      const float mu = am[j][r] + bmv;
-      const float sd = splusf(as_[j][r] + bsv);
-      if (MODE == 0) {
-        o_pm[(size_t)m * Zn + c] = mu;
-        o_ps[(size_t)m * Zn + c] = sd;
-      } else {
-        o0b[(size_t)m * Zn + c] = f2b(eps[(size_t)m * Zn + c] * sd + mu);
-        if (MODE == 1) {
-          kld += mu * mu + sd * sd - 2.0f * __logf(sd) - 1.0f;
-        } else {
-          const float pm = pm_in[(size_t)m * Zn + c];
-          const float ps = ps_in[(size_t)m * Zn + c];
-          const float dd = (mu - pm) / ps;
-          const float rr = sd / ps;
-          kld += dd * dd + rr * rr - 2.0f * __logf(rr) - 1.0f;
-        }
-      }
-    }
-  }
-  if (MODE != 0) {
-    const float s = block_sum(kld, red);
-    if (tid == 0) atomicAdd(kacc, 0.5f * s);
-  }
-}
-
-__global__ __launch_bounds__(256) void k_gemmA(
-    const us* A, const us* W, int ldw, int K, const float* bias, us* C, int ldc)
-{
-  __shared__ alignas(16) char sm[10240];
-  tile_gemmx<1, true, false, false, true>(blockIdx.x, blockIdx.y, A, W, ldw, K,
-      nullptr, nullptr, 0, 0, nullptr, 0, bias, C, ldc, sm);
-}
-
-__global__ __launch_bounds__(256) void k_gruB(
-    const us* A0, const us* Wih, const us* hprev, const us* Whh,
-    const float* bih, const float* bhh, us* hnew)
-{
-  __shared__ alignas(16) char sm[20480];
-  tile_gru_fe(blockIdx.x, blockIdx.y, A0, Wih, hprev, Whh, bih, bhh, hnew, sm);
-}
-
-__global__ __launch_bounds__(256) void k_statf(
-    const us* fh, const us* femW, const float* femb, const us* fesW, const float* fesb,
-    const float* eps_f, us* fbuf, float* kacc)
-{
-  __shared__ alignas(16) char sm[15376];
-  stat_dual<1>(blockIdx.x, fh, femW, femb, fesW, fesb, eps_f,
-               nullptr, nullptr, fbuf, nullptr, nullptr, kacc, sm);
-}
-
-__global__ __launch_bounds__(256) void kP2(
-    const us* phi_f, const us* rWih, const us* dW1, const float* db1,
-    float* Cpre_gru, float* Cpre_dec)
-{
-  __shared__ alignas(16) char sm[10240];
-  const int b = blockIdx.x;
-  if (b < 192)
-    tile_gemmx<1, false, true, false, false>(b % 24, b / 24, phi_f, rWih + 1024, 1536, Hn,
-        nullptr, nullptr, 0, 0, nullptr, 0, nullptr, Cpre_gru, 1536, sm);
-  else
-    tile_gemmx<1, false, true, false, true>((b - 192) & 7, (b - 192) >> 3,
-        phi_f, dW1 + 512, 1536, Hn,
-        nullptr, nullptr, 0, 0, nullptr, 0, db1, Cpre_dec, 512, sm);
-}
-
-__global__ __launch_bounds__(256) void kP3(
-    const us* h0, const us* zpW, const float* zpb, us* zp,
-    const us* px0, const us* zeW1, const float* zeb1, us* zepre)
-{
-  __shared__ alignas(16) char sm[10240];
-  const int b = blockIdx.x;
-  if (b < 64)
-    tile_gemmx<1, true, false, false, true>(b & 7, b >> 3, h0, zpW, Hn, Hn,
-        nullptr, nullptr, 0, 0, nullptr, 0, zpb, zp, Hn, sm);
-  else
-    tile_gemmx<2, true, false, false, true>((b - 64) & 7, (b - 64) >> 3,
-        px0, zeW1, 1024, Hn, h0, zeW1 + 512, 1024, Hn,
-        nullptr, 0, zeb1, zepre, Hn, sm);
-}
-
-__global__ __launch_bounds__(256) void kP4(
-    const us* zepre, const us* zeW2, const float* zeb2, us* ze,
-    const us* zp, const us* zpmW, const float* zpmb, const us* zpsW, const float* zpsb,
-    float* zpm, float* zps)
-{
-  __shared__ alignas(16) char sm[15376];
-  const int b = blockIdx.x;
-  if (b < 64)
-    tile_gemmx<1, true, false, false, true>(b & 7, b >> 3, zepre, zeW2, Hn, Hn,
-        nullptr, nullptr, 0, 0, nullptr, 0, zeb2, ze, Hn, sm);
-  else
-    stat_dual<0>(b - 64, zp, zpmW, zpmb, zpsW, zpsb,
-                 nullptr, nullptr, nullptr, nullptr, zpm, zps, nullptr, sm);
-}
-
-__global__ __launch_bounds__(256) void kS1(
-    const us* ze, const us* zemW, const float* zemb, const us* zesW, const float* zesb,
-    const float* eps_zt, const float* zpm, const float* zps, us* zt, float* kacc,
-    const us* px_t, const us* rWih, const float* Cpre_gru, float* gipre)
-{
-  __shared__ alignas(16) char sm[15376];
-  const int b = blockIdx.x;
-  if (b < 8)
-    stat_dual<2>(b, ze, zemW, zemb, zesW, zesb, eps_zt, zpm, zps,
-                 zt, nullptr, nullptr, kacc, sm);
-  else {
-    const int tb = b - 8;
-    tile_gemmx<1, false, true, true, false>(tb % 24, tb / 24, px_t, rWih, 1536, Hn,
-        nullptr, nullptr, 0, 0, Cpre_gru, 1536, nullptr, gipre, 1536, sm);
-  }
-}
-
-__global__ __launch_bounds__(256) void kS2(
-    const us* zt, const us* pzW, const float* pzb, us* phiz)
-{
-  __shared__ alignas(16) char sm[10240];
-  tile_gemmx<1, true, false, false, true>(blockIdx.x & 7, blockIdx.x >> 3, zt, pzW, Zn, Zn,
-      nullptr, nullptr, 0, 0, nullptr, 0, pzb, phiz, Hn, sm);
-}
-
-__global__ __launch_bounds__(256) void kS3(
-    const us* phiz, const us* rWih, const float* gipre, const float* ghpre,
-    const us* hprev, const float* rbih, const float* rbhh, us* hnew,
-    const us* dW1, const float* dtmph, us* dtmp)
-{
-  __shared__ alignas(16) char sm[20480];
-  const int b = blockIdx.x;
-  if (b < 64)
-    tile_gru_fin(b & 7, b >> 3, phiz, rWih, gipre, ghpre, hprev, rbih, rbhh, hnew, sm);
-  else
-    tile_gemmx<1, true, false, true, false>((b - 64) & 7, (b - 64) >> 3, phiz, dW1, 1536, Hn,
-        nullptr, nullptr, 0, 0, dtmph, 512, nullptr, dtmp, Hn, sm);
-}
-
-__global__ __launch_bounds__(256) void kS4(
-    const us* dtmp, const us* dW2, const float* db2, us* dec,
-    const us* hnext, const us* zpW, const float* zpb, us* zp,
-    const us* px1, const us* zeW1, const float* zeb1, us* zepre,
-    const us* dW1, const float* Cpre_dec, float* dtmph)
-{
-  __shared__ alignas(16) char sm[10240];
-  const int b = blockIdx.x;
-  if (b < 64)
-    tile_gemmx<1, true, false, false, true>(b & 7, b >> 3, dtmp, dW2, Hn, Hn,
-        nullptr, nullptr, 0, 0, nullptr, 0, db2, dec, Hn, sm);
-  else if (b < 128)
-    tile_gemmx<1, true, false, false, true>((b - 64) & 7, (b - 64) >> 3, hnext, zpW, Hn, Hn,
-        nullptr, nullptr, 0, 0, nullptr, 0, zpb, zp, Hn, sm);
-  else if (b < 192)
-    tile_gemmx<2, true, false, false, true>((b - 128) & 7, (b - 128) >> 3,
-        px1, zeW1, 1024, Hn, hnext, zeW1 + 512, 1024, Hn,
-        nullptr, 0, zeb1, zepre, Hn, sm);
-  else
-    tile_gemmx<1, false, true, true, false>((b - 192) & 7, (b - 192) >> 3,
-        hnext, dW1 + 1024, 1536, Hn,
-        nullptr, nullptr, 0, 0, Cpre_dec, 512, nullptr, dtmph, 512, sm);
-}
-
-__global__ __launch_bounds__(256) void kS5(
-    const us* dec, const us* dmW, const float* dmb, const float* xt, float* nll,
-    const us* zepre, const us* zeW2, const float* zeb2, us* ze,
-    const us* zp, const us* zpmW, const float* zpmb, const us* zpsW, const float* zpsb,
-    float* zpm, float* zps,
-    const us* hnext, const us* rWhh, float* ghpre)
-{
-  __shared__ alignas(16) char sm[15376];
-  const int b = blockIdx.x;
-  if (b < 104)
-    tile_nll(b % 13, b / 13, dec, dmW, dmb, xt, nll, sm);
-  else if (b < 168)
-    tile_gemmx<1, true, false, false, true>((b - 104) & 7, (b - 104) >> 3, zepre, zeW2, Hn, Hn,
-        nullptr, nullptr, 0, 0, nullptr, 0, zeb2, ze, Hn, sm);
-  else if (b < 176)
-    stat_dual<0>(b - 168, zp, zpmW, zpmb, zpsW, zpsb,
-                 nullptr, nullptr, nullptr, nullptr, zpm, zps, nullptr, sm);
-  else {
-    const int tb = b - 176;
-    tile_gemmx<1, false, true, false, false>(tb % 24, tb / 24, hnext, rWhh, Hn, Hn,
-        nullptr, nullptr, 0, 0, nullptr, 0, nullptr, ghpre, 1536, sm);
-  }
-}
-
 }
 
 extern "C" void kernel_launch(void* const* d_in, const int* in_sizes, int n_in,
@@ -554,192 +747,112 @@
                               hipStream_t stream)
 {
   (void)in_sizes; (void)n_in; (void)out_size;
-  const float* x     = (const float*)d_in[0];
-  const float* eps_f = (const float*)d_in[1];
-  const float* eps_z = (const float*)d_in[2];
-  const float* pxW1  = (const float*)d_in[3];
-  const float* pxb1  = (const float*)d_in[4];
-  const float* pxW2  = (const float*)d_in[5];
-  const float* pxb2  = (const float*)d_in[6];
-  const float* pzW   = (const float*)d_in[7];
-  const float* pzb   = (const float*)d_in[8];
-  const float* pfW   = (const float*)d_in[9];
-  const float* pfb   = (const float*)d_in[10];
-  const float* rWih  = (const float*)d_in[11];
-  const float* rWhh  = (const float*)d_in[12];
-  const float* rbih  = (const float*)d_in[13];
-  const float* rbhh  = (const float*)d_in[14];
-  const float* zpW   = (const float*)d_in[15];
-  const float* zpb   = (const float*)d_in[16];
-  const float* zpmW  = (const float*)d_in[17];
-  const float* zpmb  = (const float*)d_in[18];
-  const float* zpsW  = (const float*)d_in[19];
-  const float* zpsb  = (const float*)d_in[20];
-  const float* feWih = (const float*)d_in[21];
-  const float* feWhh = (const float*)d_in[22];
-  const float* febih = (const float*)d_in[23];
-  const float* febhh = (const float*)d_in[24];
-  const float* femW  = (const float*)d_in[25];
-  const float* femb  = (const float*)d_in[26];
-  const float* fesW  = (const float*)d_in[27];
-  const float* fesb  = (const float*)d_in[28];
-  const float* zeW1  = (const float*)d_in[29];
-  const float* zeb1  = (const float*)d_in[30];
-  const float* zeW2  = (const float*)d_in[31];
-  const float* zeb2  = (const float*)d_in[32];
-  const float* zemW  = (const float*)d_in[33];
-  const float* zemb  = (const float*)d_in[34];
-  const float* zesW  = (const float*)d_in[35];
-  const float* zesb  = (const float*)d_in[36];
-  const float* dW1   = (const float*)d_in[37];
-  const float* db1   = (const float*)d_in[38];
-  const float* dW2   = (const float*)d_in[39];
-  const float* db2   = (const float*)d_in[40];
-  const float* dmW   = (const float*)d_in[41];
-  const float* dmb   = (const float*)d_in[42];
-  float* out = (float*)d_out;
+  KParams p;
+  p.x      = (const float*)d_in[0];
+  p.eps_f  = (const float*)d_in[1];
+  p.eps_z  = (const float*)d_in[2];
+  p.f_pxW1 = (const float*)d_in[3];
+  p.pxb1   = (const float*)d_in[4];
+  p.f_pxW2 = (const float*)d_in[5];
+  p.pxb2   = (const float*)d_in[6];
+  p.f_pzW  = (const float*)d_in[7];
+  p.pzb    = (const float*)d_in[8];
+  p.f_pfW  = (const float*)d_in[9];
+  p.pfb    = (const float*)d_in[10];
+  p.f_rWih = (const float*)d_in[11];
+  p.f_rWhh = (const float*)d_in[12];
+  p.rbih   = (const float*)d_in[13];
+  p.rbhh   = (const float*)d_in[14];
+  p.f_zpW  = (const float*)d_in[15];
+  p.zpb    = (const float*)d_in[16];
+  p.f_zpmW = (const float*)d_in[17];
+  p.zpmb   = (const float*)d_in[18];
+  p.f_zpsW = (const float*)d_in[19];
+  p.zpsb   = (const float*)d_in[20];
+  p.f_feWih = (const float*)d_in[21];
+  p.f_feWhh = (const float*)d_in[22];
+  p.febih  = (const float*)d_in[23];
+  p.febhh  = (const float*)d_in[24];
+  p.f_femW = (const float*)d_in[25];
+  p.femb   = (const float*)d_in[26];
+  p.f_fesW = (const float*)d_in[27];
+  p.fesb   = (const float*)d_in[28];
+  p.f_zeW1 = (const float*)d_in[29];
+  p.zeb1   = (const float*)d_in[30];
+  p.f_zeW2 = (const float*)d_in[31];
+  p.zeb2   = (const float*)d_in[32];
+  p.f_zemW = (const float*)d_in[33];
+  p.zemb   = (const float*)d_in[34];
+  p.f_zesW = (const float*)d_in[35];
+  p.zesb   = (const float*)d_in[36];
+  p.f_dW1  = (const float*)d_in[37];
+  p.db1    = (const float*)d_in[38];
+  p.f_dW2  = (const float*)d_in[39];
+  p.db2    = (const float*)d_in[40];
+  p.f_dmW  = (const float*)d_in[41];
+  p.dmb    = (const float*)d_in[42];
+  p.out    = (float*)d_out;
 
   char* base = (char*)d_ws;
   size_t off = 0;
   auto ab = [&](size_t bytes) -> void* {
-    void* p = base + off;
+    void* q = base + off;
     off += (bytes + 255) & ~(size_t)255;
-    return p;
+    return q;
   };
 
-  us* b_pxW1  = (us*)ab((size_t)512 * XnP * 2);
-  us* b_pxW2  = (us*)ab((size_t)512 * 512 * 2);
-  us* b_pzW   = (us*)ab((size_t)512 * 64 * 2);
-  us* b_pfW   = (us*)ab((size_t)512 * 64 * 2);
-  us* b_rWih  = (us*)ab((size_t)1536 * 1536 * 2);
-  us* b_rWhh  = (us*)ab((size_t)1536 * 512 * 2);
-  us* b_zpW   = (us*)ab((size_t)512 * 512 * 2);
-  us* b_zpmW  = (us*)ab((size_t)64 * 512 * 2);
-  us* b_zpsW  = (us*)ab((size_t)64 * 512 * 2);
-  us* b_feWih = (us*)ab((size_t)1536 * 512 * 2);
-  us* b_feWhh = (us*)ab((size_t)1536 * 512 * 2);
-  us* b_femW  = (us*)ab((size_t)64 * 512 * 2);
-  us* b_fesW  = (us*)ab((size_t)64 * 512 * 2);
-  us* b_zeW1  = (us*)ab((size_t)512 * 1024 * 2);
-  us* b_zeW2  = (us*)ab((size_t)512 * 512 * 2);
-  us* b_zemW  = (us*)ab((size_t)64 * 512 * 2);
-  us* b_zesW  = (us*)ab((size_t)64 * 512 * 2);
-  us* b_dW1   = (us*)ab((size_t)512 * 1536 * 2);
-  us* b_dW2   = (us*)ab((size_t)512 * 512 * 2);
-  us* b_dmW   = (us*)ab((size_t)Xn * 512 * 2);
-
-  us* phi_x = (us*)ab((size_t)Tn * Bn * Hn * 2);
-  us* fh_a  = (us*)ab((size_t)Bn * Hn * 2);
-  us* h_a   = (us*)ab((size_t)Bn * Hn * 2);
-  us* fh_b  = (us*)ab((size_t)Bn * Hn * 2);
-  us* h_b   = (us*)ab((size_t)Bn * Hn * 2);
-  us* fbuf  = (us*)ab((size_t)Bn * Fn * 2);
-  us* phi_f = (us*)ab((size_t)Bn * Hn * 2);
-  us* zp    = (us*)ab((size_t)Bn * Hn * 2);
-  us* zepre = (us*)ab((size_t)Bn * Hn * 2);
-  us* ze    = (us*)ab((size_t)Bn * Hn * 2);
-  us* zt    = (us*)ab((size_t)Bn * Zn * 2);
-  us* phiz  = (us*)ab((size_t)Bn * Hn * 2);
-  us* dtmp  = (us*)ab((size_t)Bn * Hn * 2);
-  us* dec   = (us*)ab((size_t)Bn * Hn * 2);
-  float* zpm = (float*)ab((size_t)Bn * Zn * 4);
-  float* zps = (float*)ab((size_t)Bn * Zn * 4);
-  float* Cpre_gru = (float*)ab((size_t)Bn * 1536 * 4);
-  float* Cpre_dec = (float*)ab((size_t)Bn * 512 * 4);
-  float* gipre    = (float*)ab((size_t)Bn * 1536 * 4);
-  float* ghpre    = (float*)ab((size_t)Bn * 1536 * 4);
-  float* dtmph    = (float*)ab((size_t)Bn * 512 * 4);
+  p.b_pxW1  = (us*)ab((size_t)512 * XnP * 2);
+  p.b_pxW2  = (us*)ab((size_t)512 * 512 * 2);
+  p.b_pzW   = (us*)ab((size_t)512 * 64 * 2);
+  p.b_pfW   = (us*)ab((size_t)512 * 64 * 2);
+  p.b_rWih  = (us*)ab((size_t)1536 * 1536 * 2);
+  p.b_rWhh  = (us*)ab((size_t)1536 * 512 * 2);
+  p.b_zpW   = (us*)ab((size_t)512 * 512 * 2);
+  p.b_zpmW  = (us*)ab((size_t)64 * 512 * 2);
+  p.b_zpsW  = (us*)ab((size_t)64 * 512 * 2);
+  p.b_feWih = (us*)ab((size_t)1536 * 512 * 2);
+  p.b_feWhh = (us*)ab((size_t)1536 * 512 * 2);
+  p.b_femW  = (us*)ab((size_t)64 * 512 * 2);
+  p.b_fesW  = (us*)ab((size_t)64 * 512 * 2);
+  p.b_zeW1  = (us*)ab((size_t)512 * 1024 * 2);
+  p.b_zeW2  = (us*)ab((size_t)512 * 512 * 2);
+  p.b_zemW  = (us*)ab((size_t)64 * 512 * 2);
+  p.b_zesW  = (us*)ab((size_t)64 * 512 * 2);
+  p.b_dW1   = (us*)ab((size_t)512 * 1536 * 2);
+  p.b_dW2   = (us*)ab((size_t)512 * 512 * 2);
+  p.b_dmW   = (us*)ab((size_t)Xn * 512 * 2);
+
+  p.phi_x = (us*)ab((size_t)Tn * Bn * Hn * 2);
+  p.fh_a  = (us*)ab((size_t)Bn * Hn * 2);
+  p.fh_b  = (us*)ab((size_t)Bn * Hn * 2);
+  p.h_a   = (us*)ab((size_t)Bn * Hn * 2);
+  p.h_b   = (us*)ab((size_t)Bn * Hn * 2);
+  p.fbuf  = (us*)ab((size_t)Bn * Fn * 2);
+  p.phi_f = (us*)ab((size_t)Bn * Hn * 2);
+  p.zp    = (us*)ab((size_t)Bn * Hn * 2);
+  p.zepre = (us*)ab((size_t)Bn * Hn * 2);
+  p.ze    = (us*)ab((size_t)Bn * Hn * 2);
+  p.phiz  = (us*)ab((size_t)Bn * Hn * 2);
+  p.dtmp  = (us*)ab((size_t)Bn * Hn * 2);
+  p.dec   = (us*)ab((size_t)Bn * Hn * 2);
+  p.zpm = (float*)ab((size_t)Bn * Zn * 4);
+  p.zps = (float*)ab((size_t)Bn * Zn * 4);
+  p.Cpre_gru = (float*)ab((size_t)Bn * 1536 * 4);
+  p.Cpre_dec = (float*)ab((size_t)Bn * 512 * 4);
+  p.gipre    = (float*)ab((size_t)Bn * 1536 * 4);
+  p.ghpre    = (float*)ab((size_t)Bn * 1536 * 4);
+  p.dtmph    = (float*)ab((size_t)Bn * 512 * 4);
+  p.parts    = (float*)ab((size_t)16 * 4);
 
   int CH = 16;
   while (CH > 1 && off + (size_t)CH * (Bn * XnP + Bn * Hn) * 2 + 4096 > ws_size) CH >>= 1;
-  us* xch  = (us*)ab((size_t)CH * Bn * XnP * 2);
-  us* tmpb = (us*)ab((size_t)CH * Bn * Hn * 2);
-
-  hipMemsetAsync(d_out, 0, 3 * sizeof(float), stream);
-  hipMemsetAsync(fh_a, 0, 2 * (size_t)Bn * Hn * 2, stream);
-  hipMemsetAsync(ghpre, 0, (size_t)Bn * 1536 * 4, stream);
-
-  const dim3 blk(256);
-  auto CVT = [&](const float* s, us* d, size_t n) {
-    cvt<<<dim3((unsigned)((n + 255) / 256)), blk, 0, stream>>>(s, d, (int)n);
-  };
-
-  {
-    const size_t n = (size_t)512 * XnP;
-    cvt_pad<<<dim3((unsigned)((n + 255) / 256)), blk, 0, stream>>>(pxW1, b_pxW1, Xn, XnP, (int)n);
-  }
-  CVT(pxW2, b_pxW2, (size_t)512 * 512);
-  CVT(pzW, b_pzW, (size_t)512 * 64);
-  CVT(pfW, b_pfW, (size_t)512 * 64);
-  CVT(rWih, b_rWih, (size_t)1536 * 1536);
-  CVT(rWhh, b_rWhh, (size_t)1536 * 512);
-  CVT(zpW, b_zpW, (size_t)512 * 512);
-  CVT(zpmW, b_zpmW, (size_t)64 * 512);
-  CVT(zpsW, b_zpsW, (size_t)64 * 512);
-  CVT(feWih, b_feWih, (size_t)1536 * 512);
-  CVT(feWhh, b_feWhh, (size_t)1536 * 512);
-  CVT(femW, b_femW, (size_t)64 * 512);
-  CVT(fesW, b_fesW, (size_t)64 * 512);
-  CVT(zeW1, b_zeW1, (size_t)512 * 1024);
-  CVT(zeW2, b_zeW2, (size_t)512 * 512);
-  CVT(zemW, b_zemW, (size_t)64 * 512);
-  CVT(zesW, b_zesW, (size_t)64 * 512);
-  CVT(dW1, b_dW1, (size_t)512 * 1536);
-  CVT(dW2, b_dW2, (size_t)512 * 512);
-  CVT(dmW, b_dmW, (size_t)Xn * 512);
-
-  for (int c = 0; c < Tn / CH; ++c) {
-    const size_t nx = (size_t)CH * Bn * XnP;
-    cvt_pad<<<dim3((unsigned)((nx + 255) / 256)), blk, 0, stream>>>(
-        x + (size_t)c * CH * Bn * Xn, xch, Xn, XnP, (int)nx);
-    const dim3 gA(8, CH * Bn / 64);
-    k_gemmA<<<gA, blk, 0, stream>>>(xch, b_pxW1, XnP, XnP, pxb1, tmpb, Hn);
-    k_gemmA<<<gA, blk, 0, stream>>>(tmpb, b_pxW2, Hn, Hn, pxb2,
-                                    phi_x + (size_t)c * CH * Bn * Hn, Hn);
-  }
-
-  us* fc = fh_a; us* fn2 = fh_b;
-  for (int t = 0; t < Tn; ++t) {
-    k_gruB<<<dim3(8, 8), blk, 0, stream>>>(
-        phi_x + (size_t)t * Bn * Hn, b_feWih, fc, b_feWhh, febih, febhh, fn2);
-    us* sw = fc; fc = fn2; fn2 = sw;
-  }
-
-  k_statf<<<dim3(8), blk, 0, stream>>>(fh_a, b_femW, femb, b_fesW, fesb, eps_f, fbuf, out + 0);
-
-  k_gemmA<<<dim3(8, 8), blk, 0, stream>>>(fbuf, b_pfW, Fn, Fn, pfb, phi_f, Hn);
-  kP2<<<dim3(256), blk, 0, stream>>>(phi_f, b_rWih, b_dW1, db1, Cpre_gru, Cpre_dec);
-  hipMemcpyAsync(dtmph, Cpre_dec, (size_t)Bn * 512 * 4, hipMemcpyDeviceToDevice, stream);
-  kP3<<<dim3(128), blk, 0, stream>>>(h_a, b_zpW, zpb, zp, phi_x, b_zeW1, zeb1, zepre);
-  kP4<<<dim3(72), blk, 0, stream>>>(zepre, b_zeW2, zeb2, ze,
-                                    zp, b_zpmW, zpmb, b_zpsW, zpsb, zpm, zps);
-
-  for (int t = 0; t < Tn; ++t) {
-    const us* hcur = (t & 1) ? h_b : h_a;
-    us* hnext      = (t & 1) ? h_a : h_b;
-    const bool last = (t == Tn - 1);
-    const us* px_t = phi_x + (size_t)t * Bn * Hn;
-
-    kS1<<<dim3(200), blk, 0, stream>>>(
-        ze, b_zemW, zemb, b_zesW, zesb, eps_z + (size_t)t * Bn * Zn, zpm, zps,
-        zt, out + 1, px_t, b_rWih, Cpre_gru, gipre);
-
-    kS2<<<dim3(64), blk, 0, stream>>>(zt, b_pzW, pzb, phiz);
-
-    kS3<<<dim3(128), blk, 0, stream>>>(
-        phiz, b_rWih, gipre, ghpre, hcur, rbih, rbhh, hnext,
-        b_dW1, dtmph, dtmp);
-
-    kS4<<<dim3(last ? 64 : 256), blk, 0, stream>>>(
-        dtmp, b_dW2, db2, dec,
-        hnext, b_zpW, zpb, zp,
-        phi_x + (size_t)(t + 1) * Bn * Hn, b_zeW1, zeb1, zepre,
-        b_dW1, Cpre_dec, dtmph);
-
-    kS5<<<dim3(last ? 104 : 368), blk, 0, stream>>>(
-        dec, b_dmW, dmb, x + (size_t)t * Bn * Xn, out + 2,
-        zepre, b_zeW2, zeb2, ze,
-        zp, b_zpmW, zpmb, b_zpsW, zpsb, zpm, zps,
-        hnext, b_rWhh, ghpre);
-  }
-}
+  p.xch  = (us*)ab((size_t)CH * Bn * XnP * 2);
+  p.tmpb = (us*)ab((size_t)CH * Bn * Hn * 2);
+  p.CH = CH;
+
+  void* args[] = { (void*)&p };
+  hipLaunchCooperativeKernel((const void*)k_mega, dim3(NB), dim3(NTH), args, 0, stream);
+
+  k_nll_all<<<dim3(Tn * 104), dim3(NTH), 0, stream>>>(
+      p.phi_x, p.b_dmW, p.dmb, p.x, p.out + 2);
+}
```
